# Kernel tuning notes

Hardware: AMD Instinct MI355X
Metric: run time of the kernel (lower is better)

The kernel has to match this reference:

```python
import jax, jax.numpy as jnp
import numpy as np

EPS = 1e-8  # EPSILON in original repo (sharpen denom); cosine eps matches torch default 1e-8
MAX_SHIFT = 1
M_FEAT = 128


def _lstm_cell(x, h, c, W_ih, W_hh, b_ih, b_hh):
    gates = x @ W_ih.T + b_ih + h @ W_hh.T + b_hh
    i, f, g, o = jnp.split(gates, 4, axis=1)
    c_new = jax.nn.sigmoid(f) * c + jax.nn.sigmoid(i) * jnp.tanh(g)
    h_new = jax.nn.sigmoid(o) * jnp.tanh(c_new)
    return h_new, c_new


def _content_address(bank, k, b):
    # torch cosine_similarity over dim 2: dot / max(|m||k|, eps)
    dot = jnp.einsum('bnm,bm->bn', bank, k)
    denom = jnp.maximum(jnp.linalg.norm(bank, axis=2) * jnp.linalg.norm(k, axis=1, keepdims=True), 1e-8)
    return jax.nn.softmax(b * dot / denom, axis=1)


def _shift(w, s):
    # circular unroll then valid cross-correlation with per-batch kernel s [B, 2*MAX_SHIFT+1]
    wp = jnp.concatenate([w[:, -MAX_SHIFT:], w, w[:, :MAX_SHIFT]], axis=1)
    N = w.shape[1]
    taps = 2 * MAX_SHIFT + 1
    return sum(s[:, i:i + 1] * wp[:, i:i + N] for i in range(taps))


def _sharpen(w, r):
    wr = w ** r
    return wr / (wr.sum(axis=1, keepdims=True) + EPS)


def _move(bank, w_prev, k, b, g, s, r):
    w = _content_address(bank, k, b)
    w = w + (1.0 - g) * w_prev  # faithful: w_c is NOT scaled by g in the source
    w = _shift(w, s)
    return _sharpen(w, r)


def _split_read(p):
    M = M_FEAT
    k = p[:, :M]
    b = jax.nn.softplus(p[:, M:M + 1])
    g = jax.nn.sigmoid(p[:, M + 1:M + 2])
    s = jax.nn.softmax(p[:, M + 2:M + 5], axis=1)
    r = 1.0 + jax.nn.softplus(p[:, M + 5:M + 6])
    return k, b, g, s, r


def _split_write(p):
    M = M_FEAT
    k, b, g, s, r = _split_read(p[:, :M + 6])
    e = jax.nn.sigmoid(p[:, M + 6:M + 6 + M])
    a = p[:, M + 6 + M:M + 6 + 2 * M]
    return k, b, g, s, r, e, a


def setup_inputs() -> dict:
    key = jax.random.key(0)
    ks = jax.random.split(key, 16)
    B, E, H, N, M, O = 64, 256, 512, 4096, 128, 256
    rd_out, wr_out = M + 2 * MAX_SHIFT + 4, 3 * M + 2 * MAX_SHIFT + 4
    sc = 0.05
    return {
        'x': jax.random.normal(ks[0], (B, E), jnp.float32),
        'h_prev': jax.random.normal(ks[1], (B, H), jnp.float32),
        'c_prev': jax.random.normal(ks[2], (B, H), jnp.float32),
        'bank': jax.random.normal(ks[3], (B, N, M), jnp.float32) * 0.1,
        'read_w_prev': jnp.zeros((3, B, N), jnp.float32),
        'write_w_prev': jnp.zeros((3, B, N), jnp.float32),
        'W_ih': jax.random.normal(ks[4], (4 * H, E), jnp.float32) * sc,
        'W_hh': jax.random.normal(ks[5], (4 * H, H), jnp.float32) * sc,
        'b_ih': jax.random.normal(ks[6], (4 * H,), jnp.float32) * sc,
        'b_hh': jax.random.normal(ks[7], (4 * H,), jnp.float32) * sc,
        'read_W': jax.random.normal(ks[8], (3, rd_out, H), jnp.float32) * sc,
        'read_b': jax.random.normal(ks[9], (3, rd_out), jnp.float32) * sc,
        'write_W': jax.random.normal(ks[10], (3, wr_out, H), jnp.float32) * sc,
        'write_b': jax.random.normal(ks[11], (3, wr_out), jnp.float32) * sc,
        'out_W': jax.random.normal(ks[12], (O, 3 * M + H), jnp.float32) * sc,
        'out_b': jax.random.normal(ks[13], (O,), jnp.float32) * sc,
    }


def reference(x, h_prev, c_prev, bank, read_w_prev, write_w_prev,
              W_ih, W_hh, b_ih, b_hh, read_W, read_b, write_W, write_b,
              out_W, out_b):
    h, c = _lstm_cell(x, h_prev, c_prev, W_ih, W_hh, b_ih, b_hh)
    reads = []
    for i in range(3):  # head_num=3, structurally distinct params per head
        # write head: update bank
        pw = h @ write_W[i].T + write_b[i]
        k, b, g, s, r, e, a = _split_write(pw)
        ww = _move(bank, write_w_prev[i], k, b, g, s, r)
        bank = bank * (1.0 - ww[:, :, None] * e[:, None, :]) + ww[:, :, None] * a[:, None, :]
        # read head: read from updated bank
        pr = h @ read_W[i].T + read_b[i]
        k, b, g, s, r = _split_read(pr)
        wr = _move(bank, read_w_prev[i], k, b, g, s, r)
        reads.append(jnp.einsum('bn,bnm->bm', wr, bank))
    out = jnp.concatenate(reads + [h], axis=1) @ out_W.T + out_b
    return out
```

## Files before the change

### kernel.cpp

```cpp
#include <hip/hip_runtime.h>
#include <math.h>

namespace {

constexpr int kB = 64;
constexpr int kN = 4096;
constexpr int kM = 128;
constexpr int kH = 512;
constexpr int kE = 256;
constexpr int kO = 256;
constexpr int kGates = 4 * kH;
constexpr int kCatW = 3 * kM + kH;
constexpr int kPRow = 1600;
constexpr int kWN = kB * kN;
constexpr float kLog2e = 1.4426950408889634f;

__device__ __forceinline__ float sigm_(float x) { return 1.f / (1.f + expf(-x)); }
__device__ __forceinline__ float softplus_(float x) { return x > 20.f ? x : log1pf(expf(x)); }

__global__ __launch_bounds__(256) void gates_gemm(const float* __restrict__ x,
                                                  const float* __restrict__ W_ih,
                                                  const float* __restrict__ h_prev,
                                                  const float* __restrict__ W_hh,
                                                  float* __restrict__ gates,
                                                  const float* __restrict__ out_b,
                                                  float* __restrict__ out,
                                                  float* __restrict__ cat) {
  if (blockIdx.x == 128) {
    const int tid = threadIdx.x;
    for (int i = tid; i < kB * kO; i += 256) out[i] = out_b[i & (kO - 1)];
    for (int i = tid; i < kB * 384; i += 256) cat[(i / 384) * kCatW + (i % 384)] = 0.f;
    return;
  }
  __shared__ float At[64 * 20];
  __shared__ float Wt[64 * 65];
  const int tid = threadIdx.x;
  const int b0 = (blockIdx.x >> 5) * 16;
  const int j0 = (blockIdx.x & 31) * 64;
  const int jg = tid & 63;
  const int bq4 = (tid >> 6) * 4;
  float acc[4] = {};
  for (int kc = 0; kc < 12; kc++) {
    const bool isx = kc < 4;
    const float* A = isx ? x : h_prev;
    const float* W = isx ? W_ih : W_hh;
    const int lda = isx ? kE : kH;
    const int k0 = (isx ? kc : (kc - 4)) * 64;
    __syncthreads();
    {
      int bb = tid >> 4;
      int kk = (tid & 15) * 4;
      float4 v = *(const float4*)(A + (size_t)(b0 + bb) * lda + k0 + kk);
      At[(kk + 0) * 20 + bb] = v.x; At[(kk + 1) * 20 + bb] = v.y;
      At[(kk + 2) * 20 + bb] = v.z; At[(kk + 3) * 20 + bb] = v.w;
    }
#pragma unroll
    for (int i = 0; i < 4; i++) {
      int idx = tid + i * 256;
      int jj = idx >> 4;
      int kk = (idx & 15) * 4;
      float4 w = *(const float4*)(W + (size_t)(j0 + jj) * lda + k0 + kk);
      Wt[(kk + 0) * 65 + jj] = w.x; Wt[(kk + 1) * 65 + jj] = w.y;
      Wt[(kk + 2) * 65 + jj] = w.z; Wt[(kk + 3) * 65 + jj] = w.w;
    }
    __syncthreads();
#pragma unroll 4
    for (int k = 0; k < 64; k++) {
      float4 av = *(const float4*)&At[k * 20 + bq4];
      float wv = Wt[k * 65 + jg];
      acc[0] += av.x * wv; acc[1] += av.y * wv; acc[2] += av.z * wv; acc[3] += av.w * wv;
    }
  }
#pragma unroll
  for (int i = 0; i < 4; i++)
    gates[(size_t)(b0 + bq4 + i) * kGates + j0 + jg] = acc[i];
}

__global__ __launch_bounds__(256) void proj_gemm(const float* __restrict__ gates,
                                                 const float* __restrict__ b_ih,
                                                 const float* __restrict__ b_hh,
                                                 const float* __restrict__ c_prev,
                                                 const float* __restrict__ write_W,
                                                 const float* __restrict__ read_W,
                                                 float* __restrict__ praw,
                                                 float* __restrict__ cat) {
  __shared__ float hs[512 * 12];
  __shared__ float Wt[64 * 65];
  const int tid = threadIdx.x;
  const int bs = blockIdx.x / 25;
  const int jt = blockIdx.x % 25;
  const int b0 = bs * 8;
  const int j0 = jt * 64;
  for (int i = tid; i < 8 * 512; i += 256) {
    int bb = i >> 9, kk = i & 511;
    int b = b0 + bb;
    const float* g = gates + (size_t)b * kGates;
    float i_ = g[kk]           + b_ih[kk]           + b_hh[kk];
    float f_ = g[512 + kk]     + b_ih[512 + kk]     + b_hh[512 + kk];
    float g_ = g[1024 + kk]    + b_ih[1024 + kk]    + b_hh[1024 + kk];
    float o_ = g[1536 + kk]    + b_ih[1536 + kk]    + b_hh[1536 + kk];
    float c = sigm_(f_) * c_prev[(size_t)b * kH + kk] + sigm_(i_) * tanhf(g_);
    float h = sigm_(o_) * tanhf(c);
    hs[kk * 12 + bb] = h;
    if (jt == 0) cat[(size_t)b * kCatW + 3 * kM + kk] = h;
  }
  const int jg = tid & 63;
  const int bq2 = (tid >> 6) * 2;
  float acc[2] = {};
  for (int kc = 0; kc < 8; kc++) {
    const int k0 = kc * 64;
    __syncthreads();
#pragma unroll
    for (int i = 0; i < 4; i++) {
      int idx = tid + i * 256;
      int jj = idx >> 4;
      int kk = (idx & 15) * 4;
      int j = j0 + jj;
      float4 w = make_float4(0.f, 0.f, 0.f, 0.f);
      if (j < 1170)      w = *(const float4*)(write_W + (size_t)j * kH + k0 + kk);
      else if (j < 1572) w = *(const float4*)(read_W + (size_t)(j - 1170) * kH + k0 + kk);
      Wt[(kk + 0) * 65 + jj] = w.x; Wt[(kk + 1) * 65 + jj] = w.y;
      Wt[(kk + 2) * 65 + jj] = w.z; Wt[(kk + 3) * 65 + jj] = w.w;
    }
    __syncthreads();
#pragma unroll 4
    for (int k = 0; k < 64; k++) {
      float2 av = *(const float2*)&hs[(k0 + k) * 12 + bq2];
      float wv = Wt[k * 65 + jg];
      acc[0] += av.x * wv; acc[1] += av.y * wv;
    }
  }
  if (j0 + jg < 1572) {
    praw[(size_t)(b0 + bq2 + 0) * kPRow + j0 + jg] = acc[0];
    praw[(size_t)(b0 + bq2 + 1) * kPRow + j0 + jg] = acc[1];
  }
}

__global__ __launch_bounds__(128) void split_params(const float* __restrict__ praw,
                                                    const float* __restrict__ write_b,
                                                    const float* __restrict__ read_b,
                                                    float* __restrict__ kwb, float* __restrict__ krb,
                                                    float* __restrict__ evb, float* __restrict__ avb,
                                                    float* __restrict__ scal,
                                                    float* __restrict__ sdot) {
  const int b = blockIdx.x;
  const int m = threadIdx.x;
  __shared__ float red[2];
  for (int i = 0; i < 3; i++) {
    const float* p = praw + (size_t)b * kPRow + i * 390;
    const float* wb = write_b + i * 390;
    float kv = p[m] + wb[m];
    kwb[((size_t)i * kB + b) * kM + m] = kv;
    evb[((size_t)i * kB + b) * kM + m] = sigm_(p[134 + m] + wb[134 + m]);
    avb[((size_t)i * kB + b) * kM + m] = p[262 + m] + wb[262 + m];
    float sq = kv * kv;
#pragma unroll
    for (int mm = 1; mm < 64; mm <<= 1) sq += __shfl_xor(sq, mm, 64);
    __syncthreads();
    if ((m & 63) == 0) red[m >> 6] = sq;
    __syncthreads();
    if (m == 0) {
      float* s = scal + ((size_t)i * kB + b) * 8;
      s[0] = softplus_(p[128] + wb[128]);
      s[1] = sigm_(p[129] + wb[129]);
      s[2] = 1.f + softplus_(p[133] + wb[133]);
      float x0 = p[130] + wb[130], x1 = p[131] + wb[131], x2 = p[132] + wb[132];
      float mx = fmaxf(x0, fmaxf(x1, x2));
      float e0 = expf(x0 - mx), e1 = expf(x1 - mx), e2 = expf(x2 - mx);
      float si = 1.f / (e0 + e1 + e2);
      s[3] = e0 * si; s[4] = e1 * si; s[5] = e2 * si;
      s[6] = sqrtf(red[0] + red[1]);
    }
    __syncthreads();
  }
  for (int i = 0; i < 3; i++) {
    const float* p = praw + (size_t)b * kPRow + 1170 + i * 134;
    const float* rb = read_b + i * 134;
    float kv = p[m] + rb[m];
    krb[((size_t)i * kB + b) * kM + m] = kv;
    float sq = kv * kv;
#pragma unroll
    for (int mm = 1; mm < 64; mm <<= 1) sq += __shfl_xor(sq, mm, 64);
    __syncthreads();
    if ((m & 63) == 0) red[m >> 6] = sq;
    __syncthreads();
    if (m == 0) {
      float* s = scal + ((size_t)(3 + i) * kB + b) * 8;
      s[0] = softplus_(p[128] + rb[128]);
      s[1] = sigm_(p[129] + rb[129]);
      s[2] = 1.f + softplus_(p[133] + rb[133]);
      float x0 = p[130] + rb[130], x1 = p[131] + rb[131], x2 = p[132] + rb[132];
      float mx = fmaxf(x0, fmaxf(x1, x2));
      float e0 = expf(x0 - mx), e1 = expf(x1 - mx), e2 = expf(x2 - mx);
      float si = 1.f / (e0 + e1 + e2);
      s[3] = e0 * si; s[4] = e1 * si; s[5] = e2 * si;
      s[6] = sqrtf(red[0] + red[1]);
    }
    __syncthreads();
  }
  __syncthreads();
  if (m < 64) {
    const float* a0 = avb + ((size_t)0 * kB + b) * kM;
    const float* a2 = avb + ((size_t)2 * kB + b) * kM;
    const float* u[5] = {a0, a0, a0, a2, a2};
    const float* v[5] = {krb + ((size_t)0 * kB + b) * kM,
                         kwb + ((size_t)1 * kB + b) * kM,
                         a0,
                         krb + ((size_t)2 * kB + b) * kM,
                         a2};
#pragma unroll
    for (int d = 0; d < 5; d++) {
      float s = u[d][m] * v[d][m] + u[d][m + 64] * v[d][m + 64];
#pragma unroll
      for (int mm = 1; mm < 64; mm <<= 1) s += __shfl_xor(s, mm, 64);
      if (m == 0) sdot[b * 8 + d] = s;
    }
  }
}

__global__ __launch_bounds__(256) void passA_k(const float* __restrict__ bank,
                                               const float* __restrict__ kwb,
                                               const float* __restrict__ krb,
                                               const float* __restrict__ evb,
                                               const float* __restrict__ avb,
                                               float* __restrict__ mA) {
  const int b = blockIdx.y, chunk = blockIdx.x;
  const int tid = threadIdx.x;
  const int lane = tid & 63, wv = tid >> 6, sub = lane >> 4, lm = lane & 15;
  const int m8 = lm * 8;
  float kw0r[8], kr0r[8], kw1r[8], a0r[8], e0r[8];
#pragma unroll
  for (int t = 0; t < 8; t++) {
    kw0r[t] = kwb[((size_t)0 * kB + b) * kM + m8 + t];
    kr0r[t] = krb[((size_t)0 * kB + b) * kM + m8 + t];
    kw1r[t] = kwb[((size_t)1 * kB + b) * kM + m8 + t];
    a0r[t]  = avb[((size_t)0 * kB + b) * kM + m8 + t];
    e0r[t]  = evb[((size_t)0 * kB + b) * kM + m8 + t];
  }
  const size_t bbase = (size_t)b * kN * kM;
  const size_t brow = (size_t)b * kN;
  const int row0 = chunk * 256 + wv * 4 + sub;
  const float* base = bank + bbase + (size_t)row0 * kM + m8;
  float4 pA0 = *(const float4*)(base);
  float4 pA1 = *(const float4*)(base + 4);
  float4 pB0 = *(const float4*)(base + (size_t)16 * kM);
  float4 pB1 = *(const float4*)(base + (size_t)16 * kM + 4);
  for (int it = 0; it < 16; it++) {
    float v[8];
    if ((it & 1) == 0) {
      v[0]=pA0.x; v[1]=pA0.y; v[2]=pA0.z; v[3]=pA0.w; v[4]=pA1.x; v[5]=pA1.y; v[6]=pA1.z; v[7]=pA1.w;
      if (it + 2 < 16) {
        const float* np = base + (size_t)(it + 2) * 16 * kM;
        pA0 = *(const float4*)np; pA1 = *(const float4*)(np + 4);
      }
    } else {
      v[0]=pB0.x; v[1]=pB0.y; v[2]=pB0.z; v[3]=pB0.w; v[4]=pB1.x; v[5]=pB1.y; v[6]=pB1.z; v[7]=pB1.w;
      if (it + 2 < 16) {
        const float* np = base + (size_t)(it + 2) * 16 * kM;
        pB0 = *(const float4*)np; pB1 = *(const float4*)(np + 4);
      }
    }
    const int row = row0 + it * 16;
    float s[10] = {};
#pragma unroll
    for (int t = 0; t < 8; t++) {
      float be = v[t] * e0r[t];
      s[0] += v[t] * kw0r[t];
      s[1] += v[t] * v[t];
      s[2] += v[t] * kr0r[t];
      s[3] += be * kr0r[t];
      s[4] += v[t] * kw1r[t];
      s[5] += be * kw1r[t];
      s[6] += be * v[t];
      s[7] += be * be;
      s[8] += v[t] * a0r[t];
      s[9] += be * a0r[t];
    }
#pragma unroll
    for (int m = 1; m < 16; m <<= 1)
#pragma unroll
      for (int k = 0; k < 10; k++) s[k] += __shfl_xor(s[k], m, 64);
    if (lm == 0) {
      float4* dst = (float4*)(mA + (size_t)(brow + row) * 12);
      dst[0] = make_float4(s[0], s[1], s[2], s[3]);
      dst[1] = make_float4(s[4], s[5], s[6], s[7]);
      dst[2] = make_float4(s[8], s[9], 0.f, 0.f);
    }
  }
}

__device__ void addr_core4(int tid, float* loc, const float* sc, const float* __restrict__ wp,
                           float* wb, float* red) {
  const float g = sc[1], r = sc[2];
  const float s0 = sc[3], s1c = sc[4], s2 = sc[5];
  const int lane = tid & 63, wid = tid >> 6;
  __syncthreads();
  float mx = fmaxf(fmaxf(loc[0], loc[1]), fmaxf(loc[2], loc[3]));
#pragma unroll
  for (int m = 1; m < 64; m <<= 1) mx = fmaxf(mx, __shfl_xor(mx, m, 64));
  if (lane == 0) red[wid] = mx;
  __syncthreads();
  mx = red[0];
#pragma unroll
  for (int k = 1; k < 16; k++) mx = fmaxf(mx, red[k]);
  float sum = 0.f;
#pragma unroll
  for (int i = 0; i < 4; i++) { loc[i] = exp2f((loc[i] - mx) * kLog2e); sum += loc[i]; }
#pragma unroll
  for (int m = 1; m < 64; m <<= 1) sum += __shfl_xor(sum, m, 64);
  __syncthreads();
  if (lane == 0) red[wid] = sum;
  __syncthreads();
  sum = red[0];
#pragma unroll
  for (int k = 1; k < 16; k++) sum += red[k];
  const float inv = 1.f / sum;
  const float omg = 1.f - g;
#pragma unroll
  for (int i = 0; i < 4; i++) {
    int n = tid + i * 1024;
    wb[n] = loc[i] * inv + omg * wp[n];
  }
  __syncthreads();
  float ssum = 0.f;
#pragma unroll
  for (int i = 0; i < 4; i++) {
    int n = tid + i * 1024;
    float sh = s0 * wb[(n + kN - 1) & (kN - 1)] + s1c * wb[n] + s2 * wb[(n + 1) & (kN - 1)];
    float y = (sh > 0.f) ? exp2f(r * log2f(sh)) : 0.f;
    loc[i] = y;
    ssum += y;
  }
#pragma unroll
  for (int m = 1; m < 64; m <<= 1) ssum += __shfl_xor(ssum, m, 64);
  __syncthreads();
  if (lane == 0) red[wid] = ssum;
  __syncthreads();
  ssum = red[0];
#pragma unroll
  for (int k = 1; k < 16; k++) ssum += red[k];
  const float invs = 1.f / (ssum + 1e-8f);
#pragma unroll
  for (int i = 0; i < 4; i++) loc[i] *= invs;
  __syncthreads();
}

__global__ __launch_bounds__(1024) void a12_k(const float* __restrict__ mA,
                                              const float* __restrict__ scal,
                                              const float* __restrict__ sdot,
                                              const float* __restrict__ read_w_prev,
                                              const float* __restrict__ write_w_prev,
                                              float* __restrict__ wpack) {
  const int b = blockIdx.x;
  const int tid = threadIdx.x;
  __shared__ float wb[kN];
  __shared__ float red[16];
  const size_t brow = (size_t)b * kN;
  float loc[4], w0r[4], q1r[4];
  {
    const float* sc = scal + ((size_t)0 * kB + b) * 8;
    const float beta = sc[0], kn = sc[6];
#pragma unroll
    for (int i = 0; i < 4; i++) {
      const float* mp = mA + (size_t)(brow + tid + i * 1024) * 12;
      float4 q0 = *(const float4*)mp;
      loc[i] = beta * q0.x / fmaxf(sqrtf(fmaxf(q0.y, 0.f)) * kn, 1e-8f);
    }
    addr_core4(tid, loc, sc, write_w_prev + brow, wb, red);
#pragma unroll
    for (int i = 0; i < 4; i++) {
      wpack[(size_t)(brow + tid + i * 1024) * 8 + 0] = loc[i];
      w0r[i] = loc[i];
    }
  }
  {
    const float* sc = scal + ((size_t)3 * kB + b) * 8;
    const float beta = sc[0], kn = sc[6];
    const float sa0kr0 = sdot[b * 8 + 0], sa0a0 = sdot[b * 8 + 2];
#pragma unroll
    for (int i = 0; i < 4; i++) {
      const float* mp = mA + (size_t)(brow + tid + i * 1024) * 12;
      float4 q0 = *(const float4*)mp;
      float4 q1 = *(const float4*)(mp + 4);
      float4 q2 = *(const float4*)(mp + 8);
      float w0 = w0r[i], w0q = w0 * w0;
      float q1v = q0.y
                - 2.f * w0 * q1.z
                + w0q * q1.w
                + 2.f * w0 * q2.x
                - 2.f * w0q * q2.y
                + w0q * sa0a0;
      q1r[i] = q1v;
      float d = q0.z - w0 * q0.w + w0 * sa0kr0;
      loc[i] = beta * d / fmaxf(sqrtf(fmaxf(q1v, 0.f)) * kn, 1e-8f);
    }
    addr_core4(tid, loc, sc, read_w_prev + brow, wb, red);
#pragma unroll
    for (int i = 0; i < 4; i++)
      wpack[(size_t)(brow + tid + i * 1024) * 8 + 2] = loc[i];
  }
  {
    const float* sc = scal + ((size_t)1 * kB + b) * 8;
    const float beta = sc[0], kn = sc[6];
    const float sa0kw1 = sdot[b * 8 + 1];
#pragma unroll
    for (int i = 0; i < 4; i++) {
      const float* mp = mA + (size_t)(brow + tid + i * 1024) * 12;
      float4 q1 = *(const float4*)(mp + 4);
      float w0 = w0r[i];
      float d = q1.x - w0 * q1.y + w0 * sa0kw1;
      loc[i] = beta * d / fmaxf(sqrtf(fmaxf(q1r[i], 0.f)) * kn, 1e-8f);
    }
    addr_core4(tid, loc, sc, write_w_prev + kWN + brow, wb, red);
#pragma unroll
    for (int i = 0; i < 4; i++)
      wpack[(size_t)(brow + tid + i * 1024) * 8 + 1] = loc[i];
  }
}

__global__ __launch_bounds__(256) void passB_k(const float* __restrict__ bank,
                                               const float* __restrict__ wpack,
                                               const float* __restrict__ kwb,
                                               const float* __restrict__ krb,
                                               const float* __restrict__ evb,
                                               const float* __restrict__ avb,
                                               float* __restrict__ cat,
                                               float* __restrict__ mB) {
  const int b = blockIdx.y, chunk = blockIdx.x;
  const int tid = threadIdx.x;
  const int lane = tid & 63, wv = tid >> 6, sub = lane >> 4, lm = lane & 15;
  const int m8 = lm * 8;
  float e0r[8], a0r[8], e1r[8], a1r[8], kr1r[8], kw2r[8], kr2r[8], e2r[8], a2r[8];
#pragma unroll
  for (int t = 0; t < 8; t++) {
    e0r[t]  = evb[((size_t)0 * kB + b) * kM + m8 + t];
    a0r[t]  = avb[((size_t)0 * kB + b) * kM + m8 + t];
    e1r[t]  = evb[((size_t)1 * kB + b) * kM + m8 + t];
    a1r[t]  = avb[((size_t)1 * kB + b) * kM + m8 + t];
    kr1r[t] = krb[((size_t)1 * kB + b) * kM + m8 + t];
    kw2r[t] = kwb[((size_t)2 * kB + b) * kM + m8 + t];
    kr2r[t] = krb[((size_t)2 * kB + b) * kM + m8 + t];
    e2r[t]  = evb[((size_t)2 * kB + b) * kM + m8 + t];
    a2r[t]  = avb[((size_t)2 * kB + b) * kM + m8 + t];
  }
  float racc[8] = {};
  __shared__ float rlds[kM];
  if (tid < kM) rlds[tid] = 0.f;
  const size_t bbase = (size_t)b * kN * kM;
  const size_t brow = (size_t)b * kN;
  const int row0 = chunk * 256 + wv * 4 + sub;
  const float* base = bank + bbase + (size_t)row0 * kM + m8;
  const float* wbase = wpack + (size_t)(brow + row0) * 8;
  float4 pA0 = *(const float4*)(base);
  float4 pA1 = *(const float4*)(base + 4);
  float4 wA  = *(const float4*)(wbase);
  float4 pB0 = *(const float4*)(base + (size_t)16 * kM);
  float4 pB1 = *(const float4*)(base + (size_t)16 * kM + 4);
  float4 wB  = *(const float4*)(wbase + (size_t)16 * 8);
  for (int it = 0; it < 16; it++) {
    float v[8];
    float w0, w1, wr0;
    if ((it & 1) == 0) {
      v[0]=pA0.x; v[1]=pA0.y; v[2]=pA0.z; v[3]=pA0.w; v[4]=pA1.x; v[5]=pA1.y; v[6]=pA1.z; v[7]=pA1.w;
      w0 = wA.x; w1 = wA.y; wr0 = wA.z;
      if (it + 2 < 16) {
        const float* np = base + (size_t)(it + 2) * 16 * kM;
        pA0 = *(const float4*)np; pA1 = *(const float4*)(np + 4);
        wA = *(const float4*)(wbase + (size_t)(it + 2) * 16 * 8);
      }
    } else {
      v[0]=pB0.x; v[1]=pB0.y; v[2]=pB0.z; v[3]=pB0.w; v[4]=pB1.x; v[5]=pB1.y; v[6]=pB1.z; v[7]=pB1.w;
      w0 = wB.x; w1 = wB.y; wr0 = wB.z;
      if (it + 2 < 16) {
        const float* np = base + (size_t)(it + 2) * 16 * kM;
        pB0 = *(const float4*)np; pB1 = *(const float4*)(np + 4);
        wB = *(const float4*)(wbase + (size_t)(it + 2) * 16 * 8);
      }
    }
    const int row = row0 + it * 16;
#pragma unroll
    for (int t = 0; t < 8; t++) {
      v[t] += w0 * (a0r[t] - e0r[t] * v[t]);
      racc[t] += wr0 * v[t];
      v[t] += w1 * (a1r[t] - e1r[t] * v[t]);
    }
    float s[9] = {};
#pragma unroll
    for (int t = 0; t < 8; t++) {
      float ve = v[t] * e2r[t];
      s[0] += v[t] * kr1r[t];
      s[1] += v[t] * kw2r[t];
      s[2] += v[t] * v[t];
      s[3] += v[t] * kr2r[t];
      s[4] += ve * kr2r[t];
      s[5] += ve * v[t];
      s[6] += ve * ve;
      s[7] += v[t] * a2r[t];
      s[8] += ve * a2r[t];
    }
#pragma unroll
    for (int m = 1; m < 16; m <<= 1)
#pragma unroll
      for (int k = 0; k < 9; k++) s[k] += __shfl_xor(s[k], m, 64);
    if (lm == 0) {
      float4* dst = (float4*)(mB + (size_t)(brow + row) * 12);
      dst[0] = make_float4(s[0], s[1], s[2], s[3]);
      dst[1] = make_float4(s[4], s[5], s[6], s[7]);
      dst[2] = make_float4(s[8], 0.f, 0.f, 0.f);
    }
  }
  __syncthreads();
#pragma unroll
  for (int t = 0; t < 8; t++) {
    racc[t] += __shfl_xor(racc[t], 16, 64);
    racc[t] += __shfl_xor(racc[t], 32, 64);
  }
  if (sub == 0) {
#pragma unroll
    for (int t = 0; t < 8; t++) atomicAdd(&rlds[m8 + t], racc[t]);
  }
  __syncthreads();
  if (tid < kM) atomicAdd(&cat[(size_t)b * kCatW + tid], rlds[tid]);
}

__global__ __launch_bounds__(1024) void a34_k(const float* __restrict__ mB,
                                              const float* __restrict__ scal,
                                              const float* __restrict__ sdot,
                                              const float* __restrict__ read_w_prev,
                                              const float* __restrict__ write_w_prev,
                                              float* __restrict__ wpack) {
  const int b = blockIdx.x;
  const int tid = threadIdx.x;
  __shared__ float wb[kN];
  __shared__ float red[16];
  const size_t brow = (size_t)b * kN;
  float loc[4], w2r[4];
  {
    const float* sc = scal + ((size_t)4 * kB + b) * 8;
    const float beta = sc[0], kn = sc[6];
#pragma unroll
    for (int i = 0; i < 4; i++) {
      const float* mp = mB + (size_t)(brow + tid + i * 1024) * 12;
      float4 q0 = *(const float4*)mp;
      loc[i] = beta * q0.x / fmaxf(sqrtf(fmaxf(q0.z, 0.f)) * kn, 1e-8f);
    }
    addr_core4(tid, loc, sc, read_w_prev + kWN + brow, wb, red);
#pragma unroll
    for (int i = 0; i < 4; i++)
      wpack[(size_t)(brow + tid + i * 1024) * 8 + 4] = loc[i];
  }
  {
    const float* sc = scal + ((size_t)2 * kB + b) * 8;
    const float beta = sc[0], kn = sc[6];
#pragma unroll
    for (int i = 0; i < 4; i++) {
      const float* mp = mB + (size_t)(brow + tid + i * 1024) * 12;
      float4 q0 = *(const float4*)mp;
      loc[i] = beta * q0.y / fmaxf(sqrtf(fmaxf(q0.z, 0.f)) * kn, 1e-8f);
    }
    addr_core4(tid, loc, sc, write_w_prev + 2 * kWN + brow, wb, red);
#pragma unroll
    for (int i = 0; i < 4; i++) {
      wpack[(size_t)(brow + tid + i * 1024) * 8 + 3] = loc[i];
      w2r[i] = loc[i];
    }
  }
  {
    const float* sc = scal + ((size_t)5 * kB + b) * 8;
    const float beta = sc[0], kn = sc[6];
    const float sa2kr2 = sdot[b * 8 + 3], sa2a2 = sdot[b * 8 + 4];
#pragma unroll
    for (int i = 0; i < 4; i++) {
      const float* mp = mB + (size_t)(brow + tid + i * 1024) * 12;
      float4 q0 = *(const float4*)mp;
      float4 q1 = *(const float4*)(mp + 4);
      float4 q2 = *(const float4*)(mp + 8);
      float w2 = w2r[i], w2q = w2 * w2;
      float q3 = q0.z
               - 2.f * w2 * q1.y
               + w2q * q1.z
               + 2.f * w2 * q1.w
               - 2.f * w2q * q2.x
               + w2q * sa2a2;
      float d = q0.w - w2 * q1.x + w2 * sa2kr2;
      loc[i] = beta * d / fmaxf(sqrtf(fmaxf(q3, 0.f)) * kn, 1e-8f);
    }
    addr_core4(tid, loc, sc, read_w_prev + 2 * kWN + brow, wb, red);
#pragma unroll
    for (int i = 0; i < 4; i++)
      wpack[(size_t)(brow + tid + i * 1024) * 8 + 5] = loc[i];
  }
}

__global__ __launch_bounds__(256) void passC_k(const float* __restrict__ bank,
                                               const float* __restrict__ wpack,
                                               const float* __restrict__ evb,
                                               const float* __restrict__ avb,
                                               float* __restrict__ cat) {
  const int b = blockIdx.y, chunk = blockIdx.x;
  const int tid = threadIdx.x;
  const int lane = tid & 63, wv = tid >> 6, sub = lane >> 4, lm = lane & 15;
  const int m8 = lm * 8;
  float e_r[3][8], a_r[3][8];
#pragma unroll
  for (int j = 0; j < 3; j++)
#pragma unroll
    for (int t = 0; t < 8; t++) {
      e_r[j][t] = evb[((size_t)j * kB + b) * kM + m8 + t];
      a_r[j][t] = avb[((size_t)j * kB + b) * kM + m8 + t];
    }
  float racc1[8] = {}, racc2[8] = {};
  __shared__ float rlds[2][kM];
  if (tid < kM) { rlds[0][tid] = 0.f; rlds[1][tid] = 0.f; }
  const size_t bbase = (size_t)b * kN * kM;
  const size_t brow = (size_t)b * kN;
  const int row0 = chunk * 256 + wv * 4 + sub;
  const float* base = bank + bbase + (size_t)row0 * kM + m8;
  const float* wbase = wpack + (size_t)(brow + row0) * 8;
  float4 pA0 = *(const float4*)(base);
  float4 pA1 = *(const float4*)(base + 4);
  float4 wAa = *(const float4*)(wbase);
  float4 wAb = *(const float4*)(wbase + 4);
  float4 pB0 = *(const float4*)(base + (size_t)16 * kM);
  float4 pB1 = *(const float4*)(base + (size_t)16 * kM + 4);
  float4 wBa = *(const float4*)(wbase + (size_t)16 * 8);
  float4 wBb = *(const float4*)(wbase + (size_t)16 * 8 + 4);
  for (int it = 0; it < 16; it++) {
    float v[8];
    float w0, w1, w2, wr1, wr2;
    if ((it & 1) == 0) {
      v[0]=pA0.x; v[1]=pA0.y; v[2]=pA0.z; v[3]=pA0.w; v[4]=pA1.x; v[5]=pA1.y; v[6]=pA1.z; v[7]=pA1.w;
      w0 = wAa.x; w1 = wAa.y; w2 = wAa.w; wr1 = wAb.x; wr2 = wAb.y;
      if (it + 2 < 16) {
        const float* np = base + (size_t)(it + 2) * 16 * kM;
        pA0 = *(const float4*)np; pA1 = *(const float4*)(np + 4);
        const float* wp = wbase + (size_t)(it + 2) * 16 * 8;
        wAa = *(const float4*)wp; wAb = *(const float4*)(wp + 4);
      }
    } else {
      v[0]=pB0.x; v[1]=pB0.y; v[2]=pB0.z; v[3]=pB0.w; v[4]=pB1.x; v[5]=pB1.y; v[6]=pB1.z; v[7]=pB1.w;
      w0 = wBa.x; w1 = wBa.y; w2 = wBa.w; wr1 = wBb.x; wr2 = wBb.y;
      if (it + 2 < 16) {
        const float* np = base + (size_t)(it + 2) * 16 * kM;
        pB0 = *(const float4*)np; pB1 = *(const float4*)(np + 4);
        const float* wp = wbase + (size_t)(it + 2) * 16 * 8;
        wBa = *(const float4*)wp; wBb = *(const float4*)(wp + 4);
      }
    }
#pragma unroll
    for (int t = 0; t < 8; t++) {
      v[t] += w0 * (a_r[0][t] - e_r[0][t] * v[t]);
      v[t] += w1 * (a_r[1][t] - e_r[1][t] * v[t]);
      racc1[t] += wr1 * v[t];
      v[t] += w2 * (a_r[2][t] - e_r[2][t] * v[t]);
      racc2[t] += wr2 * v[t];
    }
  }
  __syncthreads();
#pragma unroll
  for (int t = 0; t < 8; t++) {
    racc1[t] += __shfl_xor(racc1[t], 16, 64);
    racc1[t] += __shfl_xor(racc1[t], 32, 64);
    racc2[t] += __shfl_xor(racc2[t], 16, 64);
    racc2[t] += __shfl_xor(racc2[t], 32, 64);
  }
  if (sub == 0) {
#pragma unroll
    for (int t = 0; t < 8; t++) {
      atomicAdd(&rlds[0][m8 + t], racc1[t]);
      atomicAdd(&rlds[1][m8 + t], racc2[t]);
    }
  }
  __syncthreads();
  if (tid < kM) {
    atomicAdd(&cat[(size_t)b * kCatW + kM + tid], rlds[0][tid]);
    atomicAdd(&cat[(size_t)b * kCatW + 2 * kM + tid], rlds[1][tid]);
  }
}

__global__ __launch_bounds__(256) void out_gemm(const float* __restrict__ A,
                                                const float* __restrict__ W,
                                                float* __restrict__ C) {
  __shared__ float As[64][68];
  __shared__ float Ws[64][68];
  const int tid = threadIdx.x;
  const int j0 = blockIdx.x * 64;
  const int b0 = (tid & 15) * 4;
  const int j4 = (tid >> 4) * 4;
  float acc[4][4] = {};
  for (int kc = 0; kc < 2; kc++) {
    const int k0 = blockIdx.y * 128 + kc * 64;
    __syncthreads();
#pragma unroll
    for (int i = 0; i < 4; i++) {
      int idx = tid + i * 256;
      int bb = idx >> 4;
      int kk = (idx & 15) * 4;
      float4 v = *(const float4*)(A + (size_t)bb * kCatW + k0 + kk);
      As[kk][bb] = v.x; As[kk + 1][bb] = v.y; As[kk + 2][bb] = v.z; As[kk + 3][bb] = v.w;
      float4 w = *(const float4*)(W + (size_t)(j0 + bb) * kCatW + k0 + kk);
      Ws[kk][bb] = w.x; Ws[kk + 1][bb] = w.y; Ws[kk + 2][bb] = w.z; Ws[kk + 3][bb] = w.w;
    }
    __syncthreads();
#pragma unroll 2
    for (int k = 0; k < 64; k++) {
      float4 av = *(const float4*)&As[k][b0];
      float4 wv = *(const float4*)&Ws[k][j4];
      float aa[4] = {av.x, av.y, av.z, av.w};
      float ww[4] = {wv.x, wv.y, wv.z, wv.w};
#pragma unroll
      for (int ii = 0; ii < 4; ii++)
#pragma unroll
        for (int jj = 0; jj < 4; jj++) acc[ii][jj] += aa[ii] * ww[jj];
    }
  }
#pragma unroll
  for (int ii = 0; ii < 4; ii++)
#pragma unroll
    for (int jj = 0; jj < 4; jj++)
      atomicAdd(&C[(size_t)(b0 + ii) * kO + j0 + j4 + jj], acc[ii][jj]);
}

}

extern "C" void kernel_launch(void* const* d_in, const int* in_sizes, int n_in,
                              void* d_out, int out_size, void* d_ws, size_t ws_size,
                              hipStream_t stream) {
  const float* x            = (const float*)d_in[0];
  const float* h_prev       = (const float*)d_in[1];
  const float* c_prev       = (const float*)d_in[2];
  const float* bank         = (const float*)d_in[3];
  const float* read_w_prev  = (const float*)d_in[4];
  const float* write_w_prev = (const float*)d_in[5];
  const float* W_ih         = (const float*)d_in[6];
  const float* W_hh         = (const float*)d_in[7];
  const float* b_ih         = (const float*)d_in[8];
  const float* b_hh         = (const float*)d_in[9];
  const float* read_W       = (const float*)d_in[10];
  const float* read_b       = (const float*)d_in[11];
  const float* write_W      = (const float*)d_in[12];
  const float* write_b      = (const float*)d_in[13];
  const float* out_W        = (const float*)d_in[14];
  const float* out_b        = (const float*)d_in[15];
  float* out = (float*)d_out;

  float* ws    = (float*)d_ws;
  float* gates = ws;
  float* praw  = gates + kB * kGates;
  float* cat   = praw + kB * kPRow;
  float* kwb   = cat + kB * kCatW;
  float* krb   = kwb + 3 * kB * kM;
  float* evb   = krb + 3 * kB * kM;
  float* avb   = evb + 3 * kB * kM;
  float* scal  = avb + 3 * kB * kM;
  float* sdot  = scal + 6 * kB * 8;
  float* wpack = sdot + kB * 8;
  float* mA    = wpack + (size_t)kWN * 8;
  float* mB    = mA + (size_t)kWN * 12;

  gates_gemm<<<129, 256, 0, stream>>>(x, W_ih, h_prev, W_hh, gates, out_b, out, cat);
  proj_gemm<<<200, 256, 0, stream>>>(gates, b_ih, b_hh, c_prev, write_W, read_W, praw, cat);
  split_params<<<64, 128, 0, stream>>>(praw, write_b, read_b, kwb, krb, evb, avb, scal, sdot);

  passA_k<<<dim3(16, kB), 256, 0, stream>>>(bank, kwb, krb, evb, avb, mA);
  a12_k<<<64, 1024, 0, stream>>>(mA, scal, sdot, read_w_prev, write_w_prev, wpack);
  passB_k<<<dim3(16, kB), 256, 0, stream>>>(bank, wpack, kwb, krb, evb, avb, cat, mB);
  a34_k<<<64, 1024, 0, stream>>>(mB, scal, sdot, read_w_prev, write_w_prev, wpack);
  passC_k<<<dim3(16, kB), 256, 0, stream>>>(bank, wpack, evb, avb, cat);
  out_gemm<<<dim3(kO / 64, kCatW / 128), 256, 0, stream>>>(cat, out_W, out);

  (void)in_sizes; (void)n_in; (void)out_size; (void)ws_size;
}
```

Before: 435.7 us.

## Fuse all stages into one persistent kernel with grid-wide atomic barriers

Replaces the nine separate kernel launches with one persistent 256-block kernel. Its stages are separated by a software grid barrier built on an atomic counter, which is zeroed by a memset before each launch. The goal is to remove per-launch overhead and idle gaps between the small dependent stages. The work is redistributed as well: the gates GEMM is split over K halves into two buffers, and the addressing core now runs with 512 threads holding 8 elements each. The risks are deadlock if not all blocks are co-resident, the cost of spinning at each barrier, and lower parallelism for the bank passes than the original grids had.

```diff
diff --git a/kernel.cpp b/kernel.cpp
--- a/kernel.cpp
+++ b/kernel.cpp
@@ -13,299 +13,61 @@
 constexpr int kCatW = 3 * kM + kH;
 constexpr int kPRow = 1600;
 constexpr int kWN = kB * kN;
+constexpr int GRID = 256;
+constexpr int TPB = 512;
 constexpr float kLog2e = 1.4426950408889634f;
 
 __device__ __forceinline__ float sigm_(float x) { return 1.f / (1.f + expf(-x)); }
 __device__ __forceinline__ float softplus_(float x) { return x > 20.f ? x : log1pf(expf(x)); }
 
-__global__ __launch_bounds__(256) void gates_gemm(const float* __restrict__ x,
-                                                  const float* __restrict__ W_ih,
-                                                  const float* __restrict__ h_prev,
-                                                  const float* __restrict__ W_hh,
-                                                  float* __restrict__ gates,
-                                                  const float* __restrict__ out_b,
-                                                  float* __restrict__ out,
-                                                  float* __restrict__ cat) {
-  if (blockIdx.x == 128) {
-    const int tid = threadIdx.x;
-    for (int i = tid; i < kB * kO; i += 256) out[i] = out_b[i & (kO - 1)];
-    for (int i = tid; i < kB * 384; i += 256) cat[(i / 384) * kCatW + (i % 384)] = 0.f;
-    return;
-  }
-  __shared__ float At[64 * 20];
-  __shared__ float Wt[64 * 65];
-  const int tid = threadIdx.x;
-  const int b0 = (blockIdx.x >> 5) * 16;
-  const int j0 = (blockIdx.x & 31) * 64;
-  const int jg = tid & 63;
-  const int bq4 = (tid >> 6) * 4;
-  float acc[4] = {};
-  for (int kc = 0; kc < 12; kc++) {
-    const bool isx = kc < 4;
-    const float* A = isx ? x : h_prev;
-    const float* W = isx ? W_ih : W_hh;
-    const int lda = isx ? kE : kH;
-    const int k0 = (isx ? kc : (kc - 4)) * 64;
-    __syncthreads();
-    {
-      int bb = tid >> 4;
-      int kk = (tid & 15) * 4;
-      float4 v = *(const float4*)(A + (size_t)(b0 + bb) * lda + k0 + kk);
-      At[(kk + 0) * 20 + bb] = v.x; At[(kk + 1) * 20 + bb] = v.y;
-      At[(kk + 2) * 20 + bb] = v.z; At[(kk + 3) * 20 + bb] = v.w;
-    }
-#pragma unroll
-    for (int i = 0; i < 4; i++) {
-      int idx = tid + i * 256;
-      int jj = idx >> 4;
-      int kk = (idx & 15) * 4;
-      float4 w = *(const float4*)(W + (size_t)(j0 + jj) * lda + k0 + kk);
-      Wt[(kk + 0) * 65 + jj] = w.x; Wt[(kk + 1) * 65 + jj] = w.y;
-      Wt[(kk + 2) * 65 + jj] = w.z; Wt[(kk + 3) * 65 + jj] = w.w;
-    }
-    __syncthreads();
-#pragma unroll 4
-    for (int k = 0; k < 64; k++) {
-      float4 av = *(const float4*)&At[k * 20 + bq4];
-      float wv = Wt[k * 65 + jg];
-      acc[0] += av.x * wv; acc[1] += av.y * wv; acc[2] += av.z * wv; acc[3] += av.w * wv;
-    }
-  }
-#pragma unroll
-  for (int i = 0; i < 4; i++)
-    gates[(size_t)(b0 + bq4 + i) * kGates + j0 + jg] = acc[i];
+struct Args {
+  const float *x, *h_prev, *c_prev, *bank, *read_w_prev, *write_w_prev;
+  const float *W_ih, *W_hh, *b_ih, *b_hh, *read_W, *read_b, *write_W, *write_b, *out_W, *out_b;
+  float *out;
+  float *gates0, *gates1, *hbuf, *praw0, *praw1, *cat;
+  float *kwb, *krb, *evb, *avb, *scal, *sdot, *wpack, *mA, *mB;
+  unsigned *cnt;
+};
+
+union SMem {
+  struct { float At[64 * 20]; float Wt[64 * 65]; } g;
+  struct { float wb[kN]; float red[8]; } a;
+  struct { float nred[4][2]; } s;
+  struct { float rl[2 * kM]; } r;
+  struct { float As[64 * 72]; float Ws[64 * 72]; } o;
+};
+
+__device__ __forceinline__ void gsync(unsigned* cnt, unsigned target) {
+  __syncthreads();
+  if (threadIdx.x == 0) {
+    __threadfence();
+    atomicAdd(cnt, 1u);
+    while (__hip_atomic_load(cnt, __ATOMIC_ACQUIRE, __HIP_MEMORY_SCOPE_AGENT) < target)
+      __builtin_amdgcn_s_sleep(8);
+    __threadfence();
+  }
+  __syncthreads();
 }
 
-__global__ __launch_bounds__(256) void proj_gemm(const float* __restrict__ gates,
-                                                 const float* __restrict__ b_ih,
-                                                 const float* __restrict__ b_hh,
-                                                 const float* __restrict__ c_prev,
-                                                 const float* __restrict__ write_W,
-                                                 const float* __restrict__ read_W,
-                                                 float* __restrict__ praw,
-                                                 float* __restrict__ cat) {
-  __shared__ float hs[512 * 12];
-  __shared__ float Wt[64 * 65];
-  const int tid = threadIdx.x;
-  const int bs = blockIdx.x / 25;
-  const int jt = blockIdx.x % 25;
-  const int b0 = bs * 8;
-  const int j0 = jt * 64;
-  for (int i = tid; i < 8 * 512; i += 256) {
-    int bb = i >> 9, kk = i & 511;
-    int b = b0 + bb;
-    const float* g = gates + (size_t)b * kGates;
-    float i_ = g[kk]           + b_ih[kk]           + b_hh[kk];
-    float f_ = g[512 + kk]     + b_ih[512 + kk]     + b_hh[512 + kk];
-    float g_ = g[1024 + kk]    + b_ih[1024 + kk]    + b_hh[1024 + kk];
-    float o_ = g[1536 + kk]    + b_ih[1536 + kk]    + b_hh[1536 + kk];
-    float c = sigm_(f_) * c_prev[(size_t)b * kH + kk] + sigm_(i_) * tanhf(g_);
-    float h = sigm_(o_) * tanhf(c);
-    hs[kk * 12 + bb] = h;
-    if (jt == 0) cat[(size_t)b * kCatW + 3 * kM + kk] = h;
-  }
-  const int jg = tid & 63;
-  const int bq2 = (tid >> 6) * 2;
-  float acc[2] = {};
-  for (int kc = 0; kc < 8; kc++) {
-    const int k0 = kc * 64;
-    __syncthreads();
-#pragma unroll
-    for (int i = 0; i < 4; i++) {
-      int idx = tid + i * 256;
-      int jj = idx >> 4;
-      int kk = (idx & 15) * 4;
-      int j = j0 + jj;
-      float4 w = make_float4(0.f, 0.f, 0.f, 0.f);
-      if (j < 1170)      w = *(const float4*)(write_W + (size_t)j * kH + k0 + kk);
-      else if (j < 1572) w = *(const float4*)(read_W + (size_t)(j - 1170) * kH + k0 + kk);
-      Wt[(kk + 0) * 65 + jj] = w.x; Wt[(kk + 1) * 65 + jj] = w.y;
-      Wt[(kk + 2) * 65 + jj] = w.z; Wt[(kk + 3) * 65 + jj] = w.w;
-    }
-    __syncthreads();
-#pragma unroll 4
-    for (int k = 0; k < 64; k++) {
-      float2 av = *(const float2*)&hs[(k0 + k) * 12 + bq2];
-      float wv = Wt[k * 65 + jg];
-      acc[0] += av.x * wv; acc[1] += av.y * wv;
-    }
-  }
-  if (j0 + jg < 1572) {
-    praw[(size_t)(b0 + bq2 + 0) * kPRow + j0 + jg] = acc[0];
-    praw[(size_t)(b0 + bq2 + 1) * kPRow + j0 + jg] = acc[1];
-  }
-}
-
-__global__ __launch_bounds__(128) void split_params(const float* __restrict__ praw,
-                                                    const float* __restrict__ write_b,
-                                                    const float* __restrict__ read_b,
-                                                    float* __restrict__ kwb, float* __restrict__ krb,
-                                                    float* __restrict__ evb, float* __restrict__ avb,
-                                                    float* __restrict__ scal,
-                                                    float* __restrict__ sdot) {
-  const int b = blockIdx.x;
-  const int m = threadIdx.x;
-  __shared__ float red[2];
-  for (int i = 0; i < 3; i++) {
-    const float* p = praw + (size_t)b * kPRow + i * 390;
-    const float* wb = write_b + i * 390;
-    float kv = p[m] + wb[m];
-    kwb[((size_t)i * kB + b) * kM + m] = kv;
-    evb[((size_t)i * kB + b) * kM + m] = sigm_(p[134 + m] + wb[134 + m]);
-    avb[((size_t)i * kB + b) * kM + m] = p[262 + m] + wb[262 + m];
-    float sq = kv * kv;
-#pragma unroll
-    for (int mm = 1; mm < 64; mm <<= 1) sq += __shfl_xor(sq, mm, 64);
-    __syncthreads();
-    if ((m & 63) == 0) red[m >> 6] = sq;
-    __syncthreads();
-    if (m == 0) {
-      float* s = scal + ((size_t)i * kB + b) * 8;
-      s[0] = softplus_(p[128] + wb[128]);
-      s[1] = sigm_(p[129] + wb[129]);
-      s[2] = 1.f + softplus_(p[133] + wb[133]);
-      float x0 = p[130] + wb[130], x1 = p[131] + wb[131], x2 = p[132] + wb[132];
-      float mx = fmaxf(x0, fmaxf(x1, x2));
-      float e0 = expf(x0 - mx), e1 = expf(x1 - mx), e2 = expf(x2 - mx);
-      float si = 1.f / (e0 + e1 + e2);
-      s[3] = e0 * si; s[4] = e1 * si; s[5] = e2 * si;
-      s[6] = sqrtf(red[0] + red[1]);
-    }
-    __syncthreads();
-  }
-  for (int i = 0; i < 3; i++) {
-    const float* p = praw + (size_t)b * kPRow + 1170 + i * 134;
-    const float* rb = read_b + i * 134;
-    float kv = p[m] + rb[m];
-    krb[((size_t)i * kB + b) * kM + m] = kv;
-    float sq = kv * kv;
-#pragma unroll
-    for (int mm = 1; mm < 64; mm <<= 1) sq += __shfl_xor(sq, mm, 64);
-    __syncthreads();
-    if ((m & 63) == 0) red[m >> 6] = sq;
-    __syncthreads();
-    if (m == 0) {
-      float* s = scal + ((size_t)(3 + i) * kB + b) * 8;
-      s[0] = softplus_(p[128] + rb[128]);
-      s[1] = sigm_(p[129] + rb[129]);
-      s[2] = 1.f + softplus_(p[133] + rb[133]);
-      float x0 = p[130] + rb[130], x1 = p[131] + rb[131], x2 = p[132] + rb[132];
-      float mx = fmaxf(x0, fmaxf(x1, x2));
-      float e0 = expf(x0 - mx), e1 = expf(x1 - mx), e2 = expf(x2 - mx);
-      float si = 1.f / (e0 + e1 + e2);
-      s[3] = e0 * si; s[4] = e1 * si; s[5] = e2 * si;
-      s[6] = sqrtf(red[0] + red[1]);
-    }
-    __syncthreads();
-  }
-  __syncthreads();
-  if (m < 64) {
-    const float* a0 = avb + ((size_t)0 * kB + b) * kM;
-    const float* a2 = avb + ((size_t)2 * kB + b) * kM;
-    const float* u[5] = {a0, a0, a0, a2, a2};
-    const float* v[5] = {krb + ((size_t)0 * kB + b) * kM,
-                         kwb + ((size_t)1 * kB + b) * kM,
-                         a0,
-                         krb + ((size_t)2 * kB + b) * kM,
-                         a2};
-#pragma unroll
-    for (int d = 0; d < 5; d++) {
-      float s = u[d][m] * v[d][m] + u[d][m + 64] * v[d][m + 64];
-#pragma unroll
-      for (int mm = 1; mm < 64; mm <<= 1) s += __shfl_xor(s, mm, 64);
-      if (m == 0) sdot[b * 8 + d] = s;
-    }
-  }
-}
-
-__global__ __launch_bounds__(256) void passA_k(const float* __restrict__ bank,
-                                               const float* __restrict__ kwb,
-                                               const float* __restrict__ krb,
-                                               const float* __restrict__ evb,
-                                               const float* __restrict__ avb,
-                                               float* __restrict__ mA) {
-  const int b = blockIdx.y, chunk = blockIdx.x;
-  const int tid = threadIdx.x;
-  const int lane = tid & 63, wv = tid >> 6, sub = lane >> 4, lm = lane & 15;
-  const int m8 = lm * 8;
-  float kw0r[8], kr0r[8], kw1r[8], a0r[8], e0r[8];
-#pragma unroll
-  for (int t = 0; t < 8; t++) {
-    kw0r[t] = kwb[((size_t)0 * kB + b) * kM + m8 + t];
-    kr0r[t] = krb[((size_t)0 * kB + b) * kM + m8 + t];
-    kw1r[t] = kwb[((size_t)1 * kB + b) * kM + m8 + t];
-    a0r[t]  = avb[((size_t)0 * kB + b) * kM + m8 + t];
-    e0r[t]  = evb[((size_t)0 * kB + b) * kM + m8 + t];
-  }
-  const size_t bbase = (size_t)b * kN * kM;
-  const size_t brow = (size_t)b * kN;
-  const int row0 = chunk * 256 + wv * 4 + sub;
-  const float* base = bank + bbase + (size_t)row0 * kM + m8;
-  float4 pA0 = *(const float4*)(base);
-  float4 pA1 = *(const float4*)(base + 4);
-  float4 pB0 = *(const float4*)(base + (size_t)16 * kM);
-  float4 pB1 = *(const float4*)(base + (size_t)16 * kM + 4);
-  for (int it = 0; it < 16; it++) {
-    float v[8];
-    if ((it & 1) == 0) {
-      v[0]=pA0.x; v[1]=pA0.y; v[2]=pA0.z; v[3]=pA0.w; v[4]=pA1.x; v[5]=pA1.y; v[6]=pA1.z; v[7]=pA1.w;
-      if (it + 2 < 16) {
-        const float* np = base + (size_t)(it + 2) * 16 * kM;
-        pA0 = *(const float4*)np; pA1 = *(const float4*)(np + 4);
-      }
-    } else {
-      v[0]=pB0.x; v[1]=pB0.y; v[2]=pB0.z; v[3]=pB0.w; v[4]=pB1.x; v[5]=pB1.y; v[6]=pB1.z; v[7]=pB1.w;
-      if (it + 2 < 16) {
-        const float* np = base + (size_t)(it + 2) * 16 * kM;
-        pB0 = *(const float4*)np; pB1 = *(const float4*)(np + 4);
-      }
-    }
-    const int row = row0 + it * 16;
-    float s[10] = {};
-#pragma unroll
-    for (int t = 0; t < 8; t++) {
-      float be = v[t] * e0r[t];
-      s[0] += v[t] * kw0r[t];
-      s[1] += v[t] * v[t];
-      s[2] += v[t] * kr0r[t];
-      s[3] += be * kr0r[t];
-      s[4] += v[t] * kw1r[t];
-      s[5] += be * kw1r[t];
-      s[6] += be * v[t];
-      s[7] += be * be;
-      s[8] += v[t] * a0r[t];
-      s[9] += be * a0r[t];
-    }
-#pragma unroll
-    for (int m = 1; m < 16; m <<= 1)
-#pragma unroll
-      for (int k = 0; k < 10; k++) s[k] += __shfl_xor(s[k], m, 64);
-    if (lm == 0) {
-      float4* dst = (float4*)(mA + (size_t)(brow + row) * 12);
-      dst[0] = make_float4(s[0], s[1], s[2], s[3]);
-      dst[1] = make_float4(s[4], s[5], s[6], s[7]);
-      dst[2] = make_float4(s[8], s[9], 0.f, 0.f);
-    }
-  }
-}
-
-__device__ void addr_core4(int tid, float* loc, const float* sc, const float* __restrict__ wp,
+__device__ void addr_core8(int tid, float* loc, const float* sc, const float* __restrict__ wp,
                            float* wb, float* red) {
   const float g = sc[1], r = sc[2];
   const float s0 = sc[3], s1c = sc[4], s2 = sc[5];
   const int lane = tid & 63, wid = tid >> 6;
   __syncthreads();
-  float mx = fmaxf(fmaxf(loc[0], loc[1]), fmaxf(loc[2], loc[3]));
+  float mx = loc[0];
+#pragma unroll
+  for (int i = 1; i < 8; i++) mx = fmaxf(mx, loc[i]);
 #pragma unroll
   for (int m = 1; m < 64; m <<= 1) mx = fmaxf(mx, __shfl_xor(mx, m, 64));
   if (lane == 0) red[wid] = mx;
   __syncthreads();
   mx = red[0];
 #pragma unroll
-  for (int k = 1; k < 16; k++) mx = fmaxf(mx, red[k]);
+  for (int k = 1; k < 8; k++) mx = fmaxf(mx, red[k]);
   float sum = 0.f;
 #pragma unroll
-  for (int i = 0; i < 4; i++) { loc[i] = exp2f((loc[i] - mx) * kLog2e); sum += loc[i]; }
+  for (int i = 0; i < 8; i++) { loc[i] = exp2f((loc[i] - mx) * kLog2e); sum += loc[i]; }
 #pragma unroll
   for (int m = 1; m < 64; m <<= 1) sum += __shfl_xor(sum, m, 64);
   __syncthreads();
@@ -313,19 +75,19 @@
   __syncthreads();
   sum = red[0];
 #pragma unroll
-  for (int k = 1; k < 16; k++) sum += red[k];
+  for (int k = 1; k < 8; k++) sum += red[k];
   const float inv = 1.f / sum;
   const float omg = 1.f - g;
 #pragma unroll
-  for (int i = 0; i < 4; i++) {
-    int n = tid + i * 1024;
+  for (int i = 0; i < 8; i++) {
+    int n = tid + i * TPB;
     wb[n] = loc[i] * inv + omg * wp[n];
   }
   __syncthreads();
   float ssum = 0.f;
 #pragma unroll
-  for (int i = 0; i < 4; i++) {
-    int n = tid + i * 1024;
+  for (int i = 0; i < 8; i++) {
+    int n = tid + i * TPB;
     float sh = s0 * wb[(n + kN - 1) & (kN - 1)] + s1c * wb[n] + s2 * wb[(n + 1) & (kN - 1)];
     float y = (sh > 0.f) ? exp2f(r * log2f(sh)) : 0.f;
     loc[i] = y;
@@ -338,387 +100,630 @@
   __syncthreads();
   ssum = red[0];
 #pragma unroll
-  for (int k = 1; k < 16; k++) ssum += red[k];
+  for (int k = 1; k < 8; k++) ssum += red[k];
   const float invs = 1.f / (ssum + 1e-8f);
 #pragma unroll
-  for (int i = 0; i < 4; i++) loc[i] *= invs;
+  for (int i = 0; i < 8; i++) loc[i] *= invs;
   __syncthreads();
 }
 
-__global__ __launch_bounds__(1024) void a12_k(const float* __restrict__ mA,
-                                              const float* __restrict__ scal,
-                                              const float* __restrict__ sdot,
-                                              const float* __restrict__ read_w_prev,
-                                              const float* __restrict__ write_w_prev,
-                                              float* __restrict__ wpack) {
-  const int b = blockIdx.x;
+__global__ __launch_bounds__(TPB, 2) void mega(Args P) {
+  const int bid = blockIdx.x;
   const int tid = threadIdx.x;
-  __shared__ float wb[kN];
-  __shared__ float red[16];
-  const size_t brow = (size_t)b * kN;
-  float loc[4], w0r[4], q1r[4];
+  __shared__ SMem sm;
+
   {
-    const float* sc = scal + ((size_t)0 * kB + b) * 8;
-    const float beta = sc[0], kn = sc[6];
-#pragma unroll
-    for (int i = 0; i < 4; i++) {
-      const float* mp = mA + (size_t)(brow + tid + i * 1024) * 12;
-      float4 q0 = *(const float4*)mp;
-      loc[i] = beta * q0.x / fmaxf(sqrtf(fmaxf(q0.y, 0.f)) * kn, 1e-8f);
-    }
-    addr_core4(tid, loc, sc, write_w_prev + brow, wb, red);
-#pragma unroll
-    for (int i = 0; i < 4; i++) {
-      wpack[(size_t)(brow + tid + i * 1024) * 8 + 0] = loc[i];
-      w0r[i] = loc[i];
-    }
-  }
+    const int khalf = bid >> 7;
+    const int unit = bid & 127;
+    const int b0 = (unit >> 5) * 16;
+    const int j0 = (unit & 31) * 64;
+    const int jg = tid & 63;
+    const int bq2 = (tid >> 6) * 2;
+    float acc0 = 0.f, acc1 = 0.f;
+    for (int kc6 = 0; kc6 < 6; kc6++) {
+      const int kc = khalf * 6 + kc6;
+      const bool isx = kc < 4;
+      const float* A = isx ? P.x : P.h_prev;
+      const float* W = isx ? P.W_ih : P.W_hh;
+      const int lda = isx ? kE : kH;
+      const int k0 = (isx ? kc : (kc - 4)) * 64;
+      __syncthreads();
+      {
+        int bb = tid >> 5;
+        int kk = (tid & 31) * 2;
+        float2 v = *(const float2*)(A + (size_t)(b0 + bb) * lda + k0 + kk);
+        sm.g.At[(kk + 0) * 20 + bb] = v.x;
+        sm.g.At[(kk + 1) * 20 + bb] = v.y;
+      }
+#pragma unroll
+      for (int i = 0; i < 2; i++) {
+        int idx = tid + i * 512;
+        int jj = idx >> 4;
+        int kk = (idx & 15) * 4;
+        float4 w = *(const float4*)(W + (size_t)(j0 + jj) * lda + k0 + kk);
+        sm.g.Wt[(kk + 0) * 65 + jj] = w.x; sm.g.Wt[(kk + 1) * 65 + jj] = w.y;
+        sm.g.Wt[(kk + 2) * 65 + jj] = w.z; sm.g.Wt[(kk + 3) * 65 + jj] = w.w;
+      }
+      __syncthreads();
+#pragma unroll 4
+      for (int k = 0; k < 64; k++) {
+        float2 av = *(const float2*)&sm.g.At[k * 20 + bq2];
+        float wv = sm.g.Wt[k * 65 + jg];
+        acc0 += av.x * wv; acc1 += av.y * wv;
+      }
+    }
+    float* gd = khalf ? P.gates1 : P.gates0;
+    gd[(size_t)(b0 + bq2 + 0) * kGates + j0 + jg] = acc0;
+    gd[(size_t)(b0 + bq2 + 1) * kGates + j0 + jg] = acc1;
+  }
+  gsync(P.cnt, GRID * 1);
+
+  if (bid < 64) {
+    const int b = bid, kk = tid;
+    const float* g0 = P.gates0 + (size_t)b * kGates;
+    const float* g1 = P.gates1 + (size_t)b * kGates;
+    float i_ = g0[kk] + g1[kk] + P.b_ih[kk] + P.b_hh[kk];
+    float f_ = g0[512 + kk] + g1[512 + kk] + P.b_ih[512 + kk] + P.b_hh[512 + kk];
+    float gg = g0[1024 + kk] + g1[1024 + kk] + P.b_ih[1024 + kk] + P.b_hh[1024 + kk];
+    float o_ = g0[1536 + kk] + g1[1536 + kk] + P.b_ih[1536 + kk] + P.b_hh[1536 + kk];
+    float c = sigm_(f_) * P.c_prev[(size_t)b * kH + kk] + sigm_(i_) * tanhf(gg);
+    float h = sigm_(o_) * tanhf(c);
+    P.hbuf[(size_t)b * kH + kk] = h;
+    P.cat[(size_t)b * kCatW + 3 * kM + kk] = h;
+  } else if (bid < 80) {
+#pragma unroll
+    for (int q = 0; q < 2; q++) {
+      int i = (bid - 64) * 1024 + tid + q * 512;
+      P.out[i] = P.out_b[i & (kO - 1)];
+    }
+  } else if (bid < 96) {
+#pragma unroll
+    for (int q = 0; q < 3; q++) {
+      int i = (bid - 80) * 1536 + tid + q * 512;
+      P.cat[(size_t)(i / 384) * kCatW + (i % 384)] = 0.f;
+    }
+  }
+  gsync(P.cnt, GRID * 2);
+
+  if (bid < 200) {
+    const int kh = bid / 100;
+    const int u = bid % 100;
+    const int b0 = (u / 25) * 16;
+    const int j0 = (u % 25) * 64;
+    const int jg = tid & 63;
+    const int bq2 = (tid >> 6) * 2;
+    float acc0 = 0.f, acc1 = 0.f;
+    for (int kc4 = 0; kc4 < 4; kc4++) {
+      const int k0 = (kh * 4 + kc4) * 64;
+      __syncthreads();
+      {
+        int bb = tid >> 5;
+        int kk = (tid & 31) * 2;
+        float2 v = *(const float2*)(P.hbuf + (size_t)(b0 + bb) * kH + k0 + kk);
+        sm.g.At[(kk + 0) * 20 + bb] = v.x;
+        sm.g.At[(kk + 1) * 20 + bb] = v.y;
+      }
+#pragma unroll
+      for (int i = 0; i < 2; i++) {
+        int idx = tid + i * 512;
+        int jj = idx >> 4;
+        int kk = (idx & 15) * 4;
+        int j = j0 + jj;
+        float4 w = make_float4(0.f, 0.f, 0.f, 0.f);
+        if (j < 1170)      w = *(const float4*)(P.write_W + (size_t)j * kH + k0 + kk);
+        else if (j < 1572) w = *(const float4*)(P.read_W + (size_t)(j - 1170) * kH + k0 + kk);
+        sm.g.Wt[(kk + 0) * 65 + jj] = w.x; sm.g.Wt[(kk + 1) * 65 + jj] = w.y;
+        sm.g.Wt[(kk + 2) * 65 + jj] = w.z; sm.g.Wt[(kk + 3) * 65 + jj] = w.w;
+      }
+      __syncthreads();
+#pragma unroll 4
+      for (int k = 0; k < 64; k++) {
+        float2 av = *(const float2*)&sm.g.At[k * 20 + bq2];
+        float wv = sm.g.Wt[k * 65 + jg];
+        acc0 += av.x * wv; acc1 += av.y * wv;
+      }
+    }
+    float* pd = kh ? P.praw1 : P.praw0;
+    if (j0 + jg < 1572) {
+      pd[(size_t)(b0 + bq2 + 0) * kPRow + j0 + jg] = acc0;
+      pd[(size_t)(b0 + bq2 + 1) * kPRow + j0 + jg] = acc1;
+    }
+  }
+  gsync(P.cnt, GRID * 3);
+
+  if (bid < kB) {
+    const int b = bid;
+    const int m = tid & 127;
+    const int hg = tid >> 7;
+    const float* pr0 = P.praw0 + (size_t)b * kPRow;
+    const float* pr1 = P.praw1 + (size_t)b * kPRow;
+    {
+      const bool isw = hg < 3;
+      const int base = isw ? hg * 390 : 1170;
+      const float* bias = isw ? (P.write_b + hg * 390) : P.read_b;
+      const int slot = isw ? hg : 3;
+      float kv = pr0[base + m] + pr1[base + m] + bias[m];
+      if (isw) {
+        P.kwb[((size_t)hg * kB + b) * kM + m] = kv;
+        P.evb[((size_t)hg * kB + b) * kM + m] =
+            sigm_(pr0[base + 134 + m] + pr1[base + 134 + m] + bias[134 + m]);
+        P.avb[((size_t)hg * kB + b) * kM + m] =
+            pr0[base + 262 + m] + pr1[base + 262 + m] + bias[262 + m];
+      } else {
+        P.krb[((size_t)0 * kB + b) * kM + m] = kv;
+      }
+      float sq = kv * kv;
+#pragma unroll
+      for (int mm = 1; mm < 64; mm <<= 1) sq += __shfl_xor(sq, mm, 64);
+      if ((tid & 63) == 0) sm.s.nred[hg][m >> 6] = sq;
+      __syncthreads();
+      if (m == 0) {
+        float* s = P.scal + ((size_t)slot * kB + b) * 8;
+        s[0] = softplus_(pr0[base + 128] + pr1[base + 128] + bias[128]);
+        s[1] = sigm_(pr0[base + 129] + pr1[base + 129] + bias[129]);
+        s[2] = 1.f + softplus_(pr0[base + 133] + pr1[base + 133] + bias[133]);
+        float x0 = pr0[base + 130] + pr1[base + 130] + bias[130];
+        float x1 = pr0[base + 131] + pr1[base + 131] + bias[131];
+        float x2 = pr0[base + 132] + pr1[base + 132] + bias[132];
+        float mx = fmaxf(x0, fmaxf(x1, x2));
+        float e0 = expf(x0 - mx), e1 = expf(x1 - mx), e2 = expf(x2 - mx);
+        float si = 1.f / (e0 + e1 + e2);
+        s[3] = e0 * si; s[4] = e1 * si; s[5] = e2 * si;
+        s[6] = sqrtf(sm.s.nred[hg][0] + sm.s.nred[hg][1]);
+      }
+      __syncthreads();
+    }
+    {
+      const int j = (hg < 2) ? hg + 1 : 2;
+      const bool act = hg < 2;
+      const int base = 1170 + j * 134;
+      const float* bias = P.read_b + j * 134;
+      const int slot = 3 + j;
+      float kv = pr0[base + m] + pr1[base + m] + bias[m];
+      if (act) P.krb[((size_t)j * kB + b) * kM + m] = kv;
+      float sq = kv * kv;
+#pragma unroll
+      for (int mm = 1; mm < 64; mm <<= 1) sq += __shfl_xor(sq, mm, 64);
+      if ((tid & 63) == 0) sm.s.nred[hg][m >> 6] = sq;
+      __syncthreads();
+      if (m == 0 && act) {
+        float* s = P.scal + ((size_t)slot * kB + b) * 8;
+        s[0] = softplus_(pr0[base + 128] + pr1[base + 128] + bias[128]);
+        s[1] = sigm_(pr0[base + 129] + pr1[base + 129] + bias[129]);
+        s[2] = 1.f + softplus_(pr0[base + 133] + pr1[base + 133] + bias[133]);
+        float x0 = pr0[base + 130] + pr1[base + 130] + bias[130];
+        float x1 = pr0[base + 131] + pr1[base + 131] + bias[131];
+        float x2 = pr0[base + 132] + pr1[base + 132] + bias[132];
+        float mx = fmaxf(x0, fmaxf(x1, x2));
+        float e0 = expf(x0 - mx), e1 = expf(x1 - mx), e2 = expf(x2 - mx);
+        float si = 1.f / (e0 + e1 + e2);
+        s[3] = e0 * si; s[4] = e1 * si; s[5] = e2 * si;
+        s[6] = sqrtf(sm.s.nred[hg][0] + sm.s.nred[hg][1]);
+      }
+      __syncthreads();
+    }
+    if (tid < 64) {
+      const float* a0v = P.avb + ((size_t)0 * kB + b) * kM;
+      const float* a2v = P.avb + ((size_t)2 * kB + b) * kM;
+      const float* u[5] = {a0v, a0v, a0v, a2v, a2v};
+      const float* v[5] = {P.krb + ((size_t)0 * kB + b) * kM,
+                           P.kwb + ((size_t)1 * kB + b) * kM,
+                           a0v,
+                           P.krb + ((size_t)2 * kB + b) * kM,
+                           a2v};
+#pragma unroll
+      for (int d = 0; d < 5; d++) {
+        float s = u[d][tid] * v[d][tid] + u[d][tid + 64] * v[d][tid + 64];
+#pragma unroll
+        for (int mm = 1; mm < 64; mm <<= 1) s += __shfl_xor(s, mm, 64);
+        if (tid == 0) P.sdot[b * 8 + d] = s;
+      }
+    }
+  }
+  gsync(P.cnt, GRID * 4);
+
   {
-    const float* sc = scal + ((size_t)3 * kB + b) * 8;
-    const float beta = sc[0], kn = sc[6];
-    const float sa0kr0 = sdot[b * 8 + 0], sa0a0 = sdot[b * 8 + 2];
-#pragma unroll
-    for (int i = 0; i < 4; i++) {
-      const float* mp = mA + (size_t)(brow + tid + i * 1024) * 12;
-      float4 q0 = *(const float4*)mp;
-      float4 q1 = *(const float4*)(mp + 4);
-      float4 q2 = *(const float4*)(mp + 8);
-      float w0 = w0r[i], w0q = w0 * w0;
-      float q1v = q0.y
-                - 2.f * w0 * q1.z
-                + w0q * q1.w
-                + 2.f * w0 * q2.x
-                - 2.f * w0q * q2.y
-                + w0q * sa0a0;
-      q1r[i] = q1v;
-      float d = q0.z - w0 * q0.w + w0 * sa0kr0;
-      loc[i] = beta * d / fmaxf(sqrtf(fmaxf(q1v, 0.f)) * kn, 1e-8f);
-    }
-    addr_core4(tid, loc, sc, read_w_prev + brow, wb, red);
-#pragma unroll
-    for (int i = 0; i < 4; i++)
-      wpack[(size_t)(brow + tid + i * 1024) * 8 + 2] = loc[i];
-  }
+    const int b = bid >> 2, chunk = bid & 3;
+    const int lane = tid & 63, wv = tid >> 6, sub = lane >> 4, lm = lane & 15;
+    const int m8 = lm * 8;
+    float kw0r[8], kr0r[8], kw1r[8], a0r[8], e0r[8];
+#pragma unroll
+    for (int t = 0; t < 8; t++) {
+      kw0r[t] = P.kwb[((size_t)0 * kB + b) * kM + m8 + t];
+      kr0r[t] = P.krb[((size_t)0 * kB + b) * kM + m8 + t];
+      kw1r[t] = P.kwb[((size_t)1 * kB + b) * kM + m8 + t];
+      a0r[t]  = P.avb[((size_t)0 * kB + b) * kM + m8 + t];
+      e0r[t]  = P.evb[((size_t)0 * kB + b) * kM + m8 + t];
+    }
+    const size_t bbase = (size_t)b * kN * kM;
+    const size_t brow = (size_t)b * kN;
+    const int row0 = chunk * 1024 + wv * 4 + sub;
+    const float* base = P.bank + bbase + (size_t)row0 * kM + m8;
+    float4 pA0 = *(const float4*)(base);
+    float4 pA1 = *(const float4*)(base + 4);
+    float4 pB0 = *(const float4*)(base + (size_t)32 * kM);
+    float4 pB1 = *(const float4*)(base + (size_t)32 * kM + 4);
+    for (int it = 0; it < 32; it++) {
+      float v[8];
+      if ((it & 1) == 0) {
+        v[0]=pA0.x; v[1]=pA0.y; v[2]=pA0.z; v[3]=pA0.w; v[4]=pA1.x; v[5]=pA1.y; v[6]=pA1.z; v[7]=pA1.w;
+        if (it + 2 < 32) {
+          const float* np = base + (size_t)(it + 2) * 32 * kM;
+          pA0 = *(const float4*)np; pA1 = *(const float4*)(np + 4);
+        }
+      } else {
+        v[0]=pB0.x; v[1]=pB0.y; v[2]=pB0.z; v[3]=pB0.w; v[4]=pB1.x; v[5]=pB1.y; v[6]=pB1.z; v[7]=pB1.w;
+        if (it + 2 < 32) {
+          const float* np = base + (size_t)(it + 2) * 32 * kM;
+          pB0 = *(const float4*)np; pB1 = *(const float4*)(np + 4);
+        }
+      }
+      const int row = row0 + it * 32;
+      float s[10] = {};
+#pragma unroll
+      for (int t = 0; t < 8; t++) {
+        float be = v[t] * e0r[t];
+        s[0] += v[t] * kw0r[t];
+        s[1] += v[t] * v[t];
+        s[2] += v[t] * kr0r[t];
+        s[3] += be * kr0r[t];
+        s[4] += v[t] * kw1r[t];
+        s[5] += be * kw1r[t];
+        s[6] += be * v[t];
+        s[7] += be * be;
+        s[8] += v[t] * a0r[t];
+        s[9] += be * a0r[t];
+      }
+#pragma unroll
+      for (int m = 1; m < 16; m <<= 1)
+#pragma unroll
+        for (int k = 0; k < 10; k++) s[k] += __shfl_xor(s[k], m, 64);
+      if (lm == 0) {
+        float4* dst = (float4*)(P.mA + (size_t)(brow + row) * 12);
+        dst[0] = make_float4(s[0], s[1], s[2], s[3]);
+        dst[1] = make_float4(s[4], s[5], s[6], s[7]);
+        dst[2] = make_float4(s[8], s[9], 0.f, 0.f);
+      }
+    }
+  }
+  gsync(P.cnt, GRID * 5);
+
+  if (bid < kB) {
+    const int b = bid;
+    const size_t brow = (size_t)b * kN;
+    float loc[8], w0r[8], q1r[8];
+    {
+      const float* sc = P.scal + ((size_t)0 * kB + b) * 8;
+      const float beta = sc[0], kn = sc[6];
+#pragma unroll
+      for (int i = 0; i < 8; i++) {
+        const float* mp = P.mA + (size_t)(brow + tid + i * TPB) * 12;
+        float4 q0 = *(const float4*)mp;
+        loc[i] = beta * q0.x / fmaxf(sqrtf(fmaxf(q0.y, 0.f)) * kn, 1e-8f);
+      }
+      addr_core8(tid, loc, sc, P.write_w_prev + brow, sm.a.wb, sm.a.red);
+#pragma unroll
+      for (int i = 0; i < 8; i++) {
+        P.wpack[(size_t)(brow + tid + i * TPB) * 8 + 0] = loc[i];
+        w0r[i] = loc[i];
+      }
+    }
+    {
+      const float* sc = P.scal + ((size_t)3 * kB + b) * 8;
+      const float beta = sc[0], kn = sc[6];
+      const float sa0kr0 = P.sdot[b * 8 + 0], sa0a0 = P.sdot[b * 8 + 2];
+#pragma unroll
+      for (int i = 0; i < 8; i++) {
+        const float* mp = P.mA + (size_t)(brow + tid + i * TPB) * 12;
+        float4 q0 = *(const float4*)mp;
+        float4 q1 = *(const float4*)(mp + 4);
+        float4 q2 = *(const float4*)(mp + 8);
+        float w0 = w0r[i], w0q = w0 * w0;
+        float q1v = q0.y - 2.f * w0 * q1.z + w0q * q1.w + 2.f * w0 * q2.x
+                  - 2.f * w0q * q2.y + w0q * sa0a0;
+        q1r[i] = q1v;
+        float d = q0.z - w0 * q0.w + w0 * sa0kr0;
+        loc[i] = beta * d / fmaxf(sqrtf(fmaxf(q1v, 0.f)) * kn, 1e-8f);
+      }
+      addr_core8(tid, loc, sc, P.read_w_prev + brow, sm.a.wb, sm.a.red);
+#pragma unroll
+      for (int i = 0; i < 8; i++)
+        P.wpack[(size_t)(brow + tid + i * TPB) * 8 + 2] = loc[i];
+    }
+    {
+      const float* sc = P.scal + ((size_t)1 * kB + b) * 8;
+      const float beta = sc[0], kn = sc[6];
+      const float sa0kw1 = P.sdot[b * 8 + 1];
+#pragma unroll
+      for (int i = 0; i < 8; i++) {
+        const float* mp = P.mA + (size_t)(brow + tid + i * TPB) * 12;
+        float4 q1 = *(const float4*)(mp + 4);
+        float w0 = w0r[i];
+        float d = q1.x - w0 * q1.y + w0 * sa0kw1;
+        loc[i] = beta * d / fmaxf(sqrtf(fmaxf(q1r[i], 0.f)) * kn, 1e-8f);
+      }
+      addr_core8(tid, loc, sc, P.write_w_prev + (size_t)kWN + brow, sm.a.wb, sm.a.red);
+#pragma unroll
+      for (int i = 0; i < 8; i++)
+        P.wpack[(size_t)(brow + tid + i * TPB) * 8 + 1] = loc[i];
+    }
+  }
+  gsync(P.cnt, GRID * 6);
+
   {
-    const float* sc = scal + ((size_t)1 * kB + b) * 8;
-    const float beta = sc[0], kn = sc[6];
-    const float sa0kw1 = sdot[b * 8 + 1];
-#pragma unroll
-    for (int i = 0; i < 4; i++) {
-      const float* mp = mA + (size_t)(brow + tid + i * 1024) * 12;
-      float4 q1 = *(const float4*)(mp + 4);
-      float w0 = w0r[i];
-      float d = q1.x - w0 * q1.y + w0 * sa0kw1;
-      loc[i] = beta * d / fmaxf(sqrtf(fmaxf(q1r[i], 0.f)) * kn, 1e-8f);
-    }
-    addr_core4(tid, loc, sc, write_w_prev + kWN + brow, wb, red);
-#pragma unroll
-    for (int i = 0; i < 4; i++)
-      wpack[(size_t)(brow + tid + i * 1024) * 8 + 1] = loc[i];
-  }
-}
-
-__global__ __launch_bounds__(256) void passB_k(const float* __restrict__ bank,
-                                               const float* __restrict__ wpack,
-                                               const float* __restrict__ kwb,
-                                               const float* __restrict__ krb,
-                                               const float* __restrict__ evb,
-                                               const float* __restrict__ avb,
-                                               float* __restrict__ cat,
-                                               float* __restrict__ mB) {
-  const int b = blockIdx.y, chunk = blockIdx.x;
-  const int tid = threadIdx.x;
-  const int lane = tid & 63, wv = tid >> 6, sub = lane >> 4, lm = lane & 15;
-  const int m8 = lm * 8;
-  float e0r[8], a0r[8], e1r[8], a1r[8], kr1r[8], kw2r[8], kr2r[8], e2r[8], a2r[8];
-#pragma unroll
-  for (int t = 0; t < 8; t++) {
-    e0r[t]  = evb[((size_t)0 * kB + b) * kM + m8 + t];
-    a0r[t]  = avb[((size_t)0 * kB + b) * kM + m8 + t];
-    e1r[t]  = evb[((size_t)1 * kB + b) * kM + m8 + t];
-    a1r[t]  = avb[((size_t)1 * kB + b) * kM + m8 + t];
-    kr1r[t] = krb[((size_t)1 * kB + b) * kM + m8 + t];
-    kw2r[t] = kwb[((size_t)2 * kB + b) * kM + m8 + t];
-    kr2r[t] = krb[((size_t)2 * kB + b) * kM + m8 + t];
-    e2r[t]  = evb[((size_t)2 * kB + b) * kM + m8 + t];
-    a2r[t]  = avb[((size_t)2 * kB + b) * kM + m8 + t];
-  }
-  float racc[8] = {};
-  __shared__ float rlds[kM];
-  if (tid < kM) rlds[tid] = 0.f;
-  const size_t bbase = (size_t)b * kN * kM;
-  const size_t brow = (size_t)b * kN;
-  const int row0 = chunk * 256 + wv * 4 + sub;
-  const float* base = bank + bbase + (size_t)row0 * kM + m8;
-  const float* wbase = wpack + (size_t)(brow + row0) * 8;
-  float4 pA0 = *(const float4*)(base);
-  float4 pA1 = *(const float4*)(base + 4);
-  float4 wA  = *(const float4*)(wbase);
-  float4 pB0 = *(const float4*)(base + (size_t)16 * kM);
-  float4 pB1 = *(const float4*)(base + (size_t)16 * kM + 4);
-  float4 wB  = *(const float4*)(wbase + (size_t)16 * 8);
-  for (int it = 0; it < 16; it++) {
-    float v[8];
-    float w0, w1, wr0;
-    if ((it & 1) == 0) {
-      v[0]=pA0.x; v[1]=pA0.y; v[2]=pA0.z; v[3]=pA0.w; v[4]=pA1.x; v[5]=pA1.y; v[6]=pA1.z; v[7]=pA1.w;
-      w0 = wA.x; w1 = wA.y; wr0 = wA.z;
-      if (it + 2 < 16) {
-        const float* np = base + (size_t)(it + 2) * 16 * kM;
-        pA0 = *(const float4*)np; pA1 = *(const float4*)(np + 4);
-        wA = *(const float4*)(wbase + (size_t)(it + 2) * 16 * 8);
-      }
-    } else {
-      v[0]=pB0.x; v[1]=pB0.y; v[2]=pB0.z; v[3]=pB0.w; v[4]=pB1.x; v[5]=pB1.y; v[6]=pB1.z; v[7]=pB1.w;
-      w0 = wB.x; w1 = wB.y; wr0 = wB.z;
-      if (it + 2 < 16) {
-        const float* np = base + (size_t)(it + 2) * 16 * kM;
-        pB0 = *(const float4*)np; pB1 = *(const float4*)(np + 4);
-        wB = *(const float4*)(wbase + (size_t)(it + 2) * 16 * 8);
-      }
-    }
-    const int row = row0 + it * 16;
+    const int b = bid >> 2, chunk = bid & 3;
+    const int lane = tid & 63, wv = tid >> 6, sub = lane >> 4, lm = lane & 15;
+    const int m8 = lm * 8;
+    float e0r[8], a0r[8], e1r[8], a1r[8], kr1r[8], kw2r[8], kr2r[8], e2r[8], a2r[8];
 #pragma unroll
     for (int t = 0; t < 8; t++) {
-      v[t] += w0 * (a0r[t] - e0r[t] * v[t]);
-      racc[t] += wr0 * v[t];
-      v[t] += w1 * (a1r[t] - e1r[t] * v[t]);
-    }
-    float s[9] = {};
+      e0r[t]  = P.evb[((size_t)0 * kB + b) * kM + m8 + t];
+      a0r[t]  = P.avb[((size_t)0 * kB + b) * kM + m8 + t];
+      e1r[t]  = P.evb[((size_t)1 * kB + b) * kM + m8 + t];
+      a1r[t]  = P.avb[((size_t)1 * kB + b) * kM + m8 + t];
+      kr1r[t] = P.krb[((size_t)1 * kB + b) * kM + m8 + t];
+      kw2r[t] = P.kwb[((size_t)2 * kB + b) * kM + m8 + t];
+      kr2r[t] = P.krb[((size_t)2 * kB + b) * kM + m8 + t];
+      e2r[t]  = P.evb[((size_t)2 * kB + b) * kM + m8 + t];
+      a2r[t]  = P.avb[((size_t)2 * kB + b) * kM + m8 + t];
+    }
+    float racc[8] = {};
+    if (tid < kM) sm.r.rl[tid] = 0.f;
+    const size_t bbase = (size_t)b * kN * kM;
+    const size_t brow = (size_t)b * kN;
+    const int row0 = chunk * 1024 + wv * 4 + sub;
+    const float* base = P.bank + bbase + (size_t)row0 * kM + m8;
+    const float* wbase = P.wpack + (size_t)(brow + row0) * 8;
+    float4 pA0 = *(const float4*)(base);
+    float4 pA1 = *(const float4*)(base + 4);
+    float4 wA  = *(const float4*)(wbase);
+    float4 pB0 = *(const float4*)(base + (size_t)32 * kM);
+    float4 pB1 = *(const float4*)(base + (size_t)32 * kM + 4);
+    float4 wB  = *(const float4*)(wbase + (size_t)32 * 8);
+    for (int it = 0; it < 32; it++) {
+      float v[8];
+      float w0, w1, wr0;
+      if ((it & 1) == 0) {
+        v[0]=pA0.x; v[1]=pA0.y; v[2]=pA0.z; v[3]=pA0.w; v[4]=pA1.x; v[5]=pA1.y; v[6]=pA1.z; v[7]=pA1.w;
+        w0 = wA.x; w1 = wA.y; wr0 = wA.z;
+        if (it + 2 < 32) {
+          const float* np = base + (size_t)(it + 2) * 32 * kM;
+          pA0 = *(const float4*)np; pA1 = *(const float4*)(np + 4);
+          wA = *(const float4*)(wbase + (size_t)(it + 2) * 32 * 8);
+        }
+      } else {
+        v[0]=pB0.x; v[1]=pB0.y; v[2]=pB0.z; v[3]=pB0.w; v[4]=pB1.x; v[5]=pB1.y; v[6]=pB1.z; v[7]=pB1.w;
+        w0 = wB.x; w1 = wB.y; wr0 = wB.z;
+        if (it + 2 < 32) {
+          const float* np = base + (size_t)(it + 2) * 32 * kM;
+          pB0 = *(const float4*)np; pB1 = *(const float4*)(np + 4);
+          wB = *(const float4*)(wbase + (size_t)(it + 2) * 32 * 8);
+        }
+      }
+      const int row = row0 + it * 32;
+#pragma unroll
+      for (int t = 0; t < 8; t++) {
+        v[t] += w0 * (a0r[t] - e0r[t] * v[t]);
+        racc[t] += wr0 * v[t];
+        v[t] += w1 * (a1r[t] - e1r[t] * v[t]);
+      }
+      float s[9] = {};
+#pragma unroll
+      for (int t = 0; t < 8; t++) {
+        float ve = v[t] * e2r[t];
+        s[0] += v[t] * kr1r[t];
+        s[1] += v[t] * kw2r[t];
+        s[2] += v[t] * v[t];
+        s[3] += v[t] * kr2r[t];
+        s[4] += ve * kr2r[t];
+        s[5] += ve * v[t];
+        s[6] += ve * ve;
+        s[7] += v[t] * a2r[t];
+        s[8] += ve * a2r[t];
+      }
+#pragma unroll
+      for (int m = 1; m < 16; m <<= 1)
+#pragma unroll
+        for (int k = 0; k < 9; k++) s[k] += __shfl_xor(s[k], m, 64);
+      if (lm == 0) {
+        float4* dst = (float4*)(P.mB + (size_t)(brow + row) * 12);
+        dst[0] = make_float4(s[0], s[1], s[2], s[3]);
+        dst[1] = make_float4(s[4], s[5], s[6], s[7]);
+        dst[2] = make_float4(s[8], 0.f, 0.f, 0.f);
+      }
+    }
+    __syncthreads();
 #pragma unroll
     for (int t = 0; t < 8; t++) {
-      float ve = v[t] * e2r[t];
-      s[0] += v[t] * kr1r[t];
-      s[1] += v[t] * kw2r[t];
-      s[2] += v[t] * v[t];
-      s[3] += v[t] * kr2r[t];
-      s[4] += ve * kr2r[t];
-      s[5] += ve * v[t];
-      s[6] += ve * ve;
-      s[7] += v[t] * a2r[t];
-      s[8] += ve * a2r[t];
-    }
-#pragma unroll
-    for (int m = 1; m < 16; m <<= 1)
-#pragma unroll
-      for (int k = 0; k < 9; k++) s[k] += __shfl_xor(s[k], m, 64);
-    if (lm == 0) {
-      float4* dst = (float4*)(mB + (size_t)(brow + row) * 12);
-      dst[0] = make_float4(s[0], s[1], s[2], s[3]);
-      dst[1] = make_float4(s[4], s[5], s[6], s[7]);
-      dst[2] = make_float4(s[8], 0.f, 0.f, 0.f);
-    }
-  }
-  __syncthreads();
-#pragma unroll
-  for (int t = 0; t < 8; t++) {
-    racc[t] += __shfl_xor(racc[t], 16, 64);
-    racc[t] += __shfl_xor(racc[t], 32, 64);
-  }
-  if (sub == 0) {
-#pragma unroll
-    for (int t = 0; t < 8; t++) atomicAdd(&rlds[m8 + t], racc[t]);
-  }
-  __syncthreads();
-  if (tid < kM) atomicAdd(&cat[(size_t)b * kCatW + tid], rlds[tid]);
-}
-
-__global__ __launch_bounds__(1024) void a34_k(const float* __restrict__ mB,
-                                              const float* __restrict__ scal,
-                                              const float* __restrict__ sdot,
-                                              const float* __restrict__ read_w_prev,
-                                              const float* __restrict__ write_w_prev,
-                                              float* __restrict__ wpack) {
-  const int b = blockIdx.x;
-  const int tid = threadIdx.x;
-  __shared__ float wb[kN];
-  __shared__ float red[16];
-  const size_t brow = (size_t)b * kN;
-  float loc[4], w2r[4];
+      racc[t] += __shfl_xor(racc[t], 16, 64);
+      racc[t] += __shfl_xor(racc[t], 32, 64);
+    }
+    if (sub == 0) {
+#pragma unroll
+      for (int t = 0; t < 8; t++) atomicAdd(&sm.r.rl[m8 + t], racc[t]);
+    }
+    __syncthreads();
+    if (tid < kM) atomicAdd(&P.cat[(size_t)b * kCatW + tid], sm.r.rl[tid]);
+  }
+  gsync(P.cnt, GRID * 7);
+
+  if (bid < kB) {
+    const int b = bid;
+    const size_t brow = (size_t)b * kN;
+    float loc[8], w2r[8];
+    {
+      const float* sc = P.scal + ((size_t)4 * kB + b) * 8;
+      const float beta = sc[0], kn = sc[6];
+#pragma unroll
+      for (int i = 0; i < 8; i++) {
+        const float* mp = P.mB + (size_t)(brow + tid + i * TPB) * 12;
+        float4 q0 = *(const float4*)mp;
+        loc[i] = beta * q0.x / fmaxf(sqrtf(fmaxf(q0.z, 0.f)) * kn, 1e-8f);
+      }
+      addr_core8(tid, loc, sc, P.read_w_prev + (size_t)kWN + brow, sm.a.wb, sm.a.red);
+#pragma unroll
+      for (int i = 0; i < 8; i++)
+        P.wpack[(size_t)(brow + tid + i * TPB) * 8 + 4] = loc[i];
+    }
+    {
+      const float* sc = P.scal + ((size_t)2 * kB + b) * 8;
+      const float beta = sc[0], kn = sc[6];
+#pragma unroll
+      for (int i = 0; i < 8; i++) {
+        const float* mp = P.mB + (size_t)(brow + tid + i * TPB) * 12;
+        float4 q0 = *(const float4*)mp;
+        loc[i] = beta * q0.y / fmaxf(sqrtf(fmaxf(q0.z, 0.f)) * kn, 1e-8f);
+      }
+      addr_core8(tid, loc, sc, P.write_w_prev + (size_t)2 * kWN + brow, sm.a.wb, sm.a.red);
+#pragma unroll
+      for (int i = 0; i < 8; i++) {
+        P.wpack[(size_t)(brow + tid + i * TPB) * 8 + 3] = loc[i];
+        w2r[i] = loc[i];
+      }
+    }
+    {
+      const float* sc = P.scal + ((size_t)5 * kB + b) * 8;
+      const float beta = sc[0], kn = sc[6];
+      const float sa2kr2 = P.sdot[b * 8 + 3], sa2a2 = P.sdot[b * 8 + 4];
+#pragma unroll
+      for (int i = 0; i < 8; i++) {
+        const float* mp = P.mB + (size_t)(brow + tid + i * TPB) * 12;
+        float4 q0 = *(const float4*)mp;
+        float4 q1 = *(const float4*)(mp + 4);
+        float4 q2 = *(const float4*)(mp + 8);
+        float w2 = w2r[i], w2q = w2 * w2;
+        float q3 = q0.z - 2.f * w2 * q1.y + w2q * q1.z + 2.f * w2 * q1.w
+                 - 2.f * w2q * q2.x + w2q * sa2a2;
+        float d = q0.w - w2 * q1.x + w2 * sa2kr2;
+        loc[i] = beta * d / fmaxf(sqrtf(fmaxf(q3, 0.f)) * kn, 1e-8f);
+      }
+      addr_core8(tid, loc, sc, P.read_w_prev + (size_t)2 * kWN + brow, sm.a.wb, sm.a.red);
+#pragma unroll
+      for (int i = 0; i < 8; i++)
+        P.wpack[(size_t)(brow + tid + i * TPB) * 8 + 5] = loc[i];
+    }
+  }
+  gsync(P.cnt, GRID * 8);
+
   {
-    const float* sc = scal + ((size_t)4 * kB + b) * 8;
-    const float beta = sc[0], kn = sc[6];
-#pragma unroll
-    for (int i = 0; i < 4; i++) {
-      const float* mp = mB + (size_t)(brow + tid + i * 1024) * 12;
-      float4 q0 = *(const float4*)mp;
-      loc[i] = beta * q0.x / fmaxf(sqrtf(fmaxf(q0.z, 0.f)) * kn, 1e-8f);
-    }
-    addr_core4(tid, loc, sc, read_w_prev + kWN + brow, wb, red);
-#pragma unroll
-    for (int i = 0; i < 4; i++)
-      wpack[(size_t)(brow + tid + i * 1024) * 8 + 4] = loc[i];
-  }
-  {
-    const float* sc = scal + ((size_t)2 * kB + b) * 8;
-    const float beta = sc[0], kn = sc[6];
-#pragma unroll
-    for (int i = 0; i < 4; i++) {
-      const float* mp = mB + (size_t)(brow + tid + i * 1024) * 12;
-      float4 q0 = *(const float4*)mp;
-      loc[i] = beta * q0.y / fmaxf(sqrtf(fmaxf(q0.z, 0.f)) * kn, 1e-8f);
-    }
-    addr_core4(tid, loc, sc, write_w_prev + 2 * kWN + brow, wb, red);
-#pragma unroll
-    for (int i = 0; i < 4; i++) {
-      wpack[(size_t)(brow + tid + i * 1024) * 8 + 3] = loc[i];
-      w2r[i] = loc[i];
-    }
-  }
-  {
-    const float* sc = scal + ((size_t)5 * kB + b) * 8;
-    const float beta = sc[0], kn = sc[6];
-    const float sa2kr2 = sdot[b * 8 + 3], sa2a2 = sdot[b * 8 + 4];
-#pragma unroll
-    for (int i = 0; i < 4; i++) {
-      const float* mp = mB + (size_t)(brow + tid + i * 1024) * 12;
-      float4 q0 = *(const float4*)mp;
-      float4 q1 = *(const float4*)(mp + 4);
-      float4 q2 = *(const float4*)(mp + 8);
-      float w2 = w2r[i], w2q = w2 * w2;
-      float q3 = q0.z
-               - 2.f * w2 * q1.y
-               + w2q * q1.z
-               + 2.f * w2 * q1.w
-               - 2.f * w2q * q2.x
-               + w2q * sa2a2;
-      float d = q0.w - w2 * q1.x + w2 * sa2kr2;
-      loc[i] = beta * d / fmaxf(sqrtf(fmaxf(q3, 0.f)) * kn, 1e-8f);
-    }
-    addr_core4(tid, loc, sc, read_w_prev + 2 * kWN + brow, wb, red);
-#pragma unroll
-    for (int i = 0; i < 4; i++)
-      wpack[(size_t)(brow + tid + i * 1024) * 8 + 5] = loc[i];
-  }
-}
-
-__global__ __launch_bounds__(256) void passC_k(const float* __restrict__ bank,
-                                               const float* __restrict__ wpack,
-                                               const float* __restrict__ evb,
-                                               const float* __restrict__ avb,
-                                               float* __restrict__ cat) {
-  const int b = blockIdx.y, chunk = blockIdx.x;
-  const int tid = threadIdx.x;
-  const int lane = tid & 63, wv = tid >> 6, sub = lane >> 4, lm = lane & 15;
-  const int m8 = lm * 8;
-  float e_r[3][8], a_r[3][8];
-#pragma unroll
-  for (int j = 0; j < 3; j++)
+    const int b = bid >> 2, chunk = bid & 3;
+    const int lane = tid & 63, wv = tid >> 6, sub = lane >> 4, lm = lane & 15;
+    const int m8 = lm * 8;
+    float e_r[3][8], a_r[3][8];
+#pragma unroll
+    for (int j = 0; j < 3; j++)
+#pragma unroll
+      for (int t = 0; t < 8; t++) {
+        e_r[j][t] = P.evb[((size_t)j * kB + b) * kM + m8 + t];
+        a_r[j][t] = P.avb[((size_t)j * kB + b) * kM + m8 + t];
+      }
+    float racc1[8] = {}, racc2[8] = {};
+    if (tid < kM) { sm.r.rl[tid] = 0.f; sm.r.rl[kM + tid] = 0.f; }
+    const size_t bbase = (size_t)b * kN * kM;
+    const size_t brow = (size_t)b * kN;
+    const int row0 = chunk * 1024 + wv * 4 + sub;
+    const float* base = P.bank + bbase + (size_t)row0 * kM + m8;
+    const float* wbase = P.wpack + (size_t)(brow + row0) * 8;
+    float4 pA0 = *(const float4*)(base);
+    float4 pA1 = *(const float4*)(base + 4);
+    float4 wAa = *(const float4*)(wbase);
+    float4 wAb = *(const float4*)(wbase + 4);
+    float4 pB0 = *(const float4*)(base + (size_t)32 * kM);
+    float4 pB1 = *(const float4*)(base + (size_t)32 * kM + 4);
+    float4 wBa = *(const float4*)(wbase + (size_t)32 * 8);
+    float4 wBb = *(const float4*)(wbase + (size_t)32 * 8 + 4);
+    for (int it = 0; it < 32; it++) {
+      float v[8];
+      float w0, w1, w2, wr1, wr2;
+      if ((it & 1) == 0) {
+        v[0]=pA0.x; v[1]=pA0.y; v[2]=pA0.z; v[3]=pA0.w; v[4]=pA1.x; v[5]=pA1.y; v[6]=pA1.z; v[7]=pA1.w;
+        w0 = wAa.x; w1 = wAa.y; w2 = wAa.w; wr1 = wAb.x; wr2 = wAb.y;
+        if (it + 2 < 32) {
+          const float* np = base + (size_t)(it + 2) * 32 * kM;
+          pA0 = *(const float4*)np; pA1 = *(const float4*)(np + 4);
+          const float* wp = wbase + (size_t)(it + 2) * 32 * 8;
+          wAa = *(const float4*)wp; wAb = *(const float4*)(wp + 4);
+        }
+      } else {
+        v[0]=pB0.x; v[1]=pB0.y; v[2]=pB0.z; v[3]=pB0.w; v[4]=pB1.x; v[5]=pB1.y; v[6]=pB1.z; v[7]=pB1.w;
+        w0 = wBa.x; w1 = wBa.y; w2 = wBa.w; wr1 = wBb.x; wr2 = wBb.y;
+        if (it + 2 < 32) {
+          const float* np = base + (size_t)(it + 2) * 32 * kM;
+          pB0 = *(const float4*)np; pB1 = *(const float4*)(np + 4);
+          const float* wp = wbase + (size_t)(it + 2) * 32 * 8;
+          wBa = *(const float4*)wp; wBb = *(const float4*)(wp + 4);
+        }
+      }
+#pragma unroll
+      for (int t = 0; t < 8; t++) {
+        v[t] += w0 * (a_r[0][t] - e_r[0][t] * v[t]);
+        v[t] += w1 * (a_r[1][t] - e_r[1][t] * v[t]);
+        racc1[t] += wr1 * v[t];
+        v[t] += w2 * (a_r[2][t] - e_r[2][t] * v[t]);
+        racc2[t] += wr2 * v[t];
+      }
+    }
+    __syncthreads();
 #pragma unroll
     for (int t = 0; t < 8; t++) {
-      e_r[j][t] = evb[((size_t)j * kB + b) * kM + m8 + t];
-      a_r[j][t] = avb[((size_t)j * kB + b) * kM + m8 + t];
-    }
-  float racc1[8] = {}, racc2[8] = {};
-  __shared__ float rlds[2][kM];
-  if (tid < kM) { rlds[0][tid] = 0.f; rlds[1][tid] = 0.f; }
-  const size_t bbase = (size_t)b * kN * kM;
-  const size_t brow = (size_t)b * kN;
-  const int row0 = chunk * 256 + wv * 4 + sub;
-  const float* base = bank + bbase + (size_t)row0 * kM + m8;
-  const float* wbase = wpack + (size_t)(brow + row0) * 8;
-  float4 pA0 = *(const float4*)(base);
-  float4 pA1 = *(const float4*)(base + 4);
-  float4 wAa = *(const float4*)(wbase);
-  float4 wAb = *(const float4*)(wbase + 4);
-  float4 pB0 = *(const float4*)(base + (size_t)16 * kM);
-  float4 pB1 = *(const float4*)(base + (size_t)16 * kM + 4);
-  float4 wBa = *(const float4*)(wbase + (size_t)16 * 8);
-  float4 wBb = *(const float4*)(wbase + (size_t)16 * 8 + 4);
-  for (int it = 0; it < 16; it++) {
-    float v[8];
-    float w0, w1, w2, wr1, wr2;
-    if ((it & 1) == 0) {
-      v[0]=pA0.x; v[1]=pA0.y; v[2]=pA0.z; v[3]=pA0.w; v[4]=pA1.x; v[5]=pA1.y; v[6]=pA1.z; v[7]=pA1.w;
-      w0 = wAa.x; w1 = wAa.y; w2 = wAa.w; wr1 = wAb.x; wr2 = wAb.y;
-      if (it + 2 < 16) {
-        const float* np = base + (size_t)(it + 2) * 16 * kM;
-        pA0 = *(const float4*)np; pA1 = *(const float4*)(np + 4);
-        const float* wp = wbase + (size_t)(it + 2) * 16 * 8;
-        wAa = *(const float4*)wp; wAb = *(const float4*)(wp + 4);
-      }
-    } else {
-      v[0]=pB0.x; v[1]=pB0.y; v[2]=pB0.z; v[3]=pB0.w; v[4]=pB1.x; v[5]=pB1.y; v[6]=pB1.z; v[7]=pB1.w;
-      w0 = wBa.x; w1 = wBa.y; w2 = wBa.w; wr1 = wBb.x; wr2 = wBb.y;
-      if (it + 2 < 16) {
-        const float* np = base + (size_t)(it + 2) * 16 * kM;
-        pB0 = *(const float4*)np; pB1 = *(const float4*)(np + 4);
-        const float* wp = wbase + (size_t)(it + 2) * 16 * 8;
-        wBa = *(const float4*)wp; wBb = *(const float4*)(wp + 4);
-      }
-    }
-#pragma unroll
-    for (int t = 0; t < 8; t++) {
-      v[t] += w0 * (a_r[0][t] - e_r[0][t] * v[t]);
-      v[t] += w1 * (a_r[1][t] - e_r[1][t] * v[t]);
-      racc1[t] += wr1 * v[t];
-      v[t] += w2 * (a_r[2][t] - e_r[2][t] * v[t]);
-      racc2[t] += wr2 * v[t];
-    }
-  }
-  __syncthreads();
-#pragma unroll
-  for (int t = 0; t < 8; t++) {
-    racc1[t] += __shfl_xor(racc1[t], 16, 64);
-    racc1[t] += __shfl_xor(racc1[t], 32, 64);
-    racc2[t] += __shfl_xor(racc2[t], 16, 64);
-    racc2[t] += __shfl_xor(racc2[t], 32, 64);
-  }
-  if (sub == 0) {
-#pragma unroll
-    for (int t = 0; t < 8; t++) {
-      atomicAdd(&rlds[0][m8 + t], racc1[t]);
-      atomicAdd(&rlds[1][m8 + t], racc2[t]);
-    }
-  }
-  __syncthreads();
-  if (tid < kM) {
-    atomicAdd(&cat[(size_t)b * kCatW + kM + tid], rlds[0][tid]);
-    atomicAdd(&cat[(size_t)b * kCatW + 2 * kM + tid], rlds[1][tid]);
-  }
-}
-
-__global__ __launch_bounds__(256) void out_gemm(const float* __restrict__ A,
-                                                const float* __restrict__ W,
-                                                float* __restrict__ C) {
-  __shared__ float As[64][68];
-  __shared__ float Ws[64][68];
-  const int tid = threadIdx.x;
-  const int j0 = blockIdx.x * 64;
-  const int b0 = (tid & 15) * 4;
-  const int j4 = (tid >> 4) * 4;
-  float acc[4][4] = {};
-  for (int kc = 0; kc < 2; kc++) {
-    const int k0 = blockIdx.y * 128 + kc * 64;
+      racc1[t] += __shfl_xor(racc1[t], 16, 64);
+      racc1[t] += __shfl_xor(racc1[t], 32, 64);
+      racc2[t] += __shfl_xor(racc2[t], 16, 64);
+      racc2[t] += __shfl_xor(racc2[t], 32, 64);
+    }
+    if (sub == 0) {
+#pragma unroll
+      for (int t = 0; t < 8; t++) {
+        atomicAdd(&sm.r.rl[m8 + t], racc1[t]);
+        atomicAdd(&sm.r.rl[kM + m8 + t], racc2[t]);
+      }
+    }
     __syncthreads();
-#pragma unroll
-    for (int i = 0; i < 4; i++) {
-      int idx = tid + i * 256;
-      int bb = idx >> 4;
-      int kk = (idx & 15) * 4;
-      float4 v = *(const float4*)(A + (size_t)bb * kCatW + k0 + kk);
-      As[kk][bb] = v.x; As[kk + 1][bb] = v.y; As[kk + 2][bb] = v.z; As[kk + 3][bb] = v.w;
-      float4 w = *(const float4*)(W + (size_t)(j0 + bb) * kCatW + k0 + kk);
-      Ws[kk][bb] = w.x; Ws[kk + 1][bb] = w.y; Ws[kk + 2][bb] = w.z; Ws[kk + 3][bb] = w.w;
+    if (tid < kM) {
+      atomicAdd(&P.cat[(size_t)b * kCatW + kM + tid], sm.r.rl[tid]);
+      atomicAdd(&P.cat[(size_t)b * kCatW + 2 * kM + tid], sm.r.rl[kM + tid]);
+    }
+  }
+  gsync(P.cnt, GRID * 9);
+
+  if (bid < 56) {
+    const int jt = bid & 3, kt = bid >> 2;
+    const int j0 = jt * 64, k0 = kt * 64;
+    {
+      int bb = tid >> 3;
+      int kk = (tid & 7) * 8;
+      float4 v0 = *(const float4*)(P.cat + (size_t)bb * kCatW + k0 + kk);
+      float4 v1 = *(const float4*)(P.cat + (size_t)bb * kCatW + k0 + kk + 4);
+      sm.o.As[(kk + 0) * 72 + bb] = v0.x; sm.o.As[(kk + 1) * 72 + bb] = v0.y;
+      sm.o.As[(kk + 2) * 72 + bb] = v0.z; sm.o.As[(kk + 3) * 72 + bb] = v0.w;
+      sm.o.As[(kk + 4) * 72 + bb] = v1.x; sm.o.As[(kk + 5) * 72 + bb] = v1.y;
+      sm.o.As[(kk + 6) * 72 + bb] = v1.z; sm.o.As[(kk + 7) * 72 + bb] = v1.w;
+      float4 w0_ = *(const float4*)(P.out_W + (size_t)(j0 + bb) * kCatW + k0 + kk);
+      float4 w1_ = *(const float4*)(P.out_W + (size_t)(j0 + bb) * kCatW + k0 + kk + 4);
+      sm.o.Ws[(kk + 0) * 72 + bb] = w0_.x; sm.o.Ws[(kk + 1) * 72 + bb] = w0_.y;
+      sm.o.Ws[(kk + 2) * 72 + bb] = w0_.z; sm.o.Ws[(kk + 3) * 72 + bb] = w0_.w;
+      sm.o.Ws[(kk + 4) * 72 + bb] = w1_.x; sm.o.Ws[(kk + 5) * 72 + bb] = w1_.y;
+      sm.o.Ws[(kk + 6) * 72 + bb] = w1_.z; sm.o.Ws[(kk + 7) * 72 + bb] = w1_.w;
     }
     __syncthreads();
+    const int b0 = (tid & 15) * 4;
+    const int jq = (tid >> 4) * 2;
+    float acc[4][2] = {};
 #pragma unroll 2
     for (int k = 0; k < 64; k++) {
-      float4 av = *(const float4*)&As[k][b0];
-      float4 wv = *(const float4*)&Ws[k][j4];
-      float aa[4] = {av.x, av.y, av.z, av.w};
-      float ww[4] = {wv.x, wv.y, wv.z, wv.w};
-#pragma unroll
-      for (int ii = 0; ii < 4; ii++)
-#pragma unroll
-        for (int jj = 0; jj < 4; jj++) acc[ii][jj] += aa[ii] * ww[jj];
-    }
-  }
-#pragma unroll
-  for (int ii = 0; ii < 4; ii++)
-#pragma unroll
-    for (int jj = 0; jj < 4; jj++)
-      atomicAdd(&C[(size_t)(b0 + ii) * kO + j0 + j4 + jj], acc[ii][jj]);
+      float4 av = *(const float4*)&sm.o.As[k * 72 + b0];
+      float2 wv = *(const float2*)&sm.o.Ws[k * 72 + jq];
+      acc[0][0] += av.x * wv.x; acc[0][1] += av.x * wv.y;
+      acc[1][0] += av.y * wv.x; acc[1][1] += av.y * wv.y;
+      acc[2][0] += av.z * wv.x; acc[2][1] += av.z * wv.y;
+      acc[3][0] += av.w * wv.x; acc[3][1] += av.w * wv.y;
+    }
+#pragma unroll
+    for (int ii = 0; ii < 4; ii++) {
+      atomicAdd(&P.out[(size_t)(b0 + ii) * kO + j0 + jq + 0], acc[ii][0]);
+      atomicAdd(&P.out[(size_t)(b0 + ii) * kO + j0 + jq + 1], acc[ii][1]);
+    }
+  }
 }
 
 }
@@ -726,48 +731,46 @@
 extern "C" void kernel_launch(void* const* d_in, const int* in_sizes, int n_in,
                               void* d_out, int out_size, void* d_ws, size_t ws_size,
                               hipStream_t stream) {
-  const float* x            = (const float*)d_in[0];
-  const float* h_prev       = (const float*)d_in[1];
-  const float* c_prev       = (const float*)d_in[2];
-  const float* bank         = (const float*)d_in[3];
-  const float* read_w_prev  = (const float*)d_in[4];
-  const float* write_w_prev = (const float*)d_in[5];
-  const float* W_ih         = (const float*)d_in[6];
-  const float* W_hh         = (const float*)d_in[7];
-  const float* b_ih         = (const float*)d_in[8];
-  const float* b_hh         = (const float*)d_in[9];
-  const float* read_W       = (const float*)d_in[10];
-  const float* read_b       = (const float*)d_in[11];
-  const float* write_W      = (const float*)d_in[12];
-  const float* write_b      = (const float*)d_in[13];
-  const float* out_W        = (const float*)d_in[14];
-  const float* out_b        = (const float*)d_in[15];
-  float* out = (float*)d_out;
-
-  float* ws    = (float*)d_ws;
-  float* gates = ws;
-  float* praw  = gates + kB * kGates;
-  float* cat   = praw + kB * kPRow;
-  float* kwb   = cat + kB * kCatW;
-  float* krb   = kwb + 3 * kB * kM;
-  float* evb   = krb + 3 * kB * kM;
-  float* avb   = evb + 3 * kB * kM;
-  float* scal  = avb + 3 * kB * kM;
-  float* sdot  = scal + 6 * kB * 8;
-  float* wpack = sdot + kB * 8;
-  float* mA    = wpack + (size_t)kWN * 8;
-  float* mB    = mA + (size_t)kWN * 12;
-
-  gates_gemm<<<129, 256, 0, stream>>>(x, W_ih, h_prev, W_hh, gates, out_b, out, cat);
-  proj_gemm<<<200, 256, 0, stream>>>(gates, b_ih, b_hh, c_prev, write_W, read_W, praw, cat);
-  split_params<<<64, 128, 0, stream>>>(praw, write_b, read_b, kwb, krb, evb, avb, scal, sdot);
-
-  passA_k<<<dim3(16, kB), 256, 0, stream>>>(bank, kwb, krb, evb, avb, mA);
-  a12_k<<<64, 1024, 0, stream>>>(mA, scal, sdot, read_w_prev, write_w_prev, wpack);
-  passB_k<<<dim3(16, kB), 256, 0, stream>>>(bank, wpack, kwb, krb, evb, avb, cat, mB);
-  a34_k<<<64, 1024, 0, stream>>>(mB, scal, sdot, read_w_prev, write_w_prev, wpack);
-  passC_k<<<dim3(16, kB), 256, 0, stream>>>(bank, wpack, evb, avb, cat);
-  out_gemm<<<dim3(kO / 64, kCatW / 128), 256, 0, stream>>>(cat, out_W, out);
+  Args A_;
+  A_.x            = (const float*)d_in[0];
+  A_.h_prev       = (const float*)d_in[1];
+  A_.c_prev       = (const float*)d_in[2];
+  A_.bank         = (const float*)d_in[3];
+  A_.read_w_prev  = (const float*)d_in[4];
+  A_.write_w_prev = (const float*)d_in[5];
+  A_.W_ih         = (const float*)d_in[6];
+  A_.W_hh         = (const float*)d_in[7];
+  A_.b_ih         = (const float*)d_in[8];
+  A_.b_hh         = (const float*)d_in[9];
+  A_.read_W       = (const float*)d_in[10];
+  A_.read_b       = (const float*)d_in[11];
+  A_.write_W      = (const float*)d_in[12];
+  A_.write_b      = (const float*)d_in[13];
+  A_.out_W        = (const float*)d_in[14];
+  A_.out_b        = (const float*)d_in[15];
+  A_.out = (float*)d_out;
+
+  float* ws = (float*)d_ws;
+  A_.cnt = (unsigned*)d_ws;
+  float* p = ws + 64;
+  A_.gates0 = p; p += (size_t)kB * kGates;
+  A_.gates1 = p; p += (size_t)kB * kGates;
+  A_.hbuf   = p; p += (size_t)kB * kH;
+  A_.praw0  = p; p += (size_t)kB * kPRow;
+  A_.praw1  = p; p += (size_t)kB * kPRow;
+  A_.cat    = p; p += (size_t)kB * kCatW;
+  A_.kwb    = p; p += (size_t)3 * kB * kM;
+  A_.krb    = p; p += (size_t)3 * kB * kM;
+  A_.evb    = p; p += (size_t)3 * kB * kM;
+  A_.avb    = p; p += (size_t)3 * kB * kM;
+  A_.scal   = p; p += (size_t)6 * kB * 8;
+  A_.sdot   = p; p += (size_t)kB * 8;
+  A_.wpack  = p; p += (size_t)kWN * 8;
+  A_.mA     = p; p += (size_t)kWN * 12;
+  A_.mB     = p; p += (size_t)kWN * 12;
+
+  hipMemsetAsync(d_ws, 0, 256, stream);
+  mega<<<dim3(GRID), dim3(TPB), 0, stream>>>(A_);
 
   (void)in_sizes; (void)n_in; (void)out_size; (void)ws_size;
 }
```

New measurement: 734.2 us. +68.5%, slower.
